# Optimization experiments

Measured on AMD Instinct MI355X. Metric: run time of the kernel, lower is better.

The kernel has to match this reference:

```python
import jax, jax.numpy as jnp
import numpy as np

B, S, D_IN, D_MODEL = 128, 2048, 512, 2048
M, NSY, H, T = 25, 64, 8, 10
REP = NSY * (NSY + 1) // 2
OUT_DIMS = S * 2
DH = D_IN // H
IU, JU = np.triu_indices(NSY)
IDX_OUT = np.arange(NSY)                      # 'first-last': first n neurons for out sync
IDX_ACT = np.arange(D_MODEL - NSY, D_MODEL)   # last n neurons for action sync


def _ln(x, g, b):
    mu = x.mean(-1, keepdims=True)
    var = x.var(-1, keepdims=True)
    return (x - mu) / jnp.sqrt(var + 1e-5) * g + b


def _sync(act, alpha, beta, r, idx):
    # pairwise upper-triangle outer product without materializing (B,n,n)
    sel = act[:, idx]
    pair = sel[:, IU] * sel[:, JU]  # (B, REP)
    if alpha is None:
        alpha, beta = pair, jnp.ones_like(pair)
    else:
        alpha = r * alpha + pair
        beta = r * beta + 1.0
    return alpha / jnp.sqrt(beta), alpha, beta


def _forward(tokens, emb, W_pos, b_pos, Wq, bq, Wk, bk, Wv, bv, Wo, bo, Ws, bs,
             ln_s_g, ln_s_b, ln_n_g, ln_n_b, Wn, bn, temp, Wout, bout,
             start_act, start_trace, decay_action, decay_out):
    # rotary-style learned positional embedding: rotate [0,1] by theta in [0,180deg]
    thetas = jnp.deg2rad(jnp.linspace(0.0, 180.0, S))
    rotated = jnp.stack([-jnp.sin(thetas), jnp.cos(thetas)], -1)  # (S,2)
    pe = rotated @ W_pos + b_pos                                   # (S, D_IN)
    feats = emb[tokens] + pe[None]                                 # (B,S,D_IN)
    kh = (feats @ Wk + bk).reshape(B, S, H, DH)
    vh = (feats @ Wv + bv).reshape(B, S, H, DH)
    r_a = jnp.exp(-decay_action)[None]
    r_o = jnp.exp(-decay_out)[None]
    act = jnp.broadcast_to(start_act[None], (B, D_MODEL))
    trace = jnp.broadcast_to(start_trace[None], (B, D_MODEL, M))
    a_a = b_a = a_o = b_o = None
    preds, certs = [], []
    for _ in range(T):
        s_act, a_a, b_a = _sync(act, a_a, b_a, r_a, IDX_ACT)
        q = (s_act @ Wq + bq).reshape(B, H, DH)
        scores = jnp.einsum('bhd,bshd->bhs', q, kh) / np.float32(np.sqrt(DH))
        attn = jax.nn.softmax(scores, -1)
        o = jnp.einsum('bhs,bshd->bhd', attn, vh).reshape(B, D_IN) @ Wo + bo
        # SynapseNet: Linear -> GLU -> LayerNorm
        pre = jnp.concatenate([o, act], -1) @ Ws + bs
        g1, g2 = jnp.split(pre, 2, -1)
        state = _ln(g1 * jax.nn.sigmoid(g2), ln_s_g, ln_s_b)  # (B, D_MODEL)
        trace = jnp.concatenate([trace[:, :, 1:], state[:, :, None]], -1)
        # NLM: per-neuron linear over memory, GLU, temperature
        xn = _ln(trace, ln_n_g, ln_n_b)
        y = jnp.einsum('bnm,mon->bno', xn, Wn) + bn  # (B, D_MODEL, 2)
        act = (y[..., 0] * jax.nn.sigmoid(y[..., 1])) / temp
        s_out, a_o, b_o = _sync(act, a_o, b_o, r_o, IDX_OUT)
        pred = s_out @ Wout + bout  # (B, OUT_DIMS)
        preds.append(pred)
        logits = pred.reshape(B, S, 2)
        p = jax.nn.softmax(logits, -1)
        ent = -(p * jax.nn.log_softmax(logits, -1)).sum(-1) / np.float32(np.log(2.0))
        ne = ent.mean(-1)
        certs.append(jnp.stack([ne, 1.0 - ne], -1))
    return jnp.stack(preds, -1), jnp.stack(certs, -1)  # (B,OUT_DIMS,T),(B,2,T)


def setup_inputs() -> dict:
    key = jax.random.key(0)
    ks = jax.random.split(key, 16)
    def n(k, shape, s=0.02):
        return (jax.random.normal(k, shape) * s).astype(jnp.float32)
    bound = 1.0 / np.sqrt(M + 2)
    return {
        'tokens': jax.random.randint(ks[0], (B, S), 0, 2, dtype=jnp.int32),
        'emb': n(ks[1], (2, D_IN), 1.0),
        'W_pos': n(ks[2], (2, D_IN)), 'b_pos': jnp.zeros((D_IN,)),
        'Wq': n(ks[3], (REP, D_IN)), 'bq': jnp.zeros((D_IN,)),
        'Wk': n(ks[4], (D_IN, D_IN)), 'bk': jnp.zeros((D_IN,)),
        'Wv': n(ks[5], (D_IN, D_IN)), 'bv': jnp.zeros((D_IN,)),
        'Wo': n(ks[6], (D_IN, D_IN)), 'bo': jnp.zeros((D_IN,)),
        'Ws': n(ks[7], (D_IN + D_MODEL, 2 * D_MODEL)), 'bs': jnp.zeros((2 * D_MODEL,)),
        'ln_s_g': jnp.ones((D_MODEL,)), 'ln_s_b': jnp.zeros((D_MODEL,)),
        'ln_n_g': jnp.ones((M,)), 'ln_n_b': jnp.zeros((M,)),
        'Wn': jax.random.uniform(ks[8], (M, 2, D_MODEL), minval=-bound, maxval=bound),
        'bn': jnp.zeros((1, D_MODEL, 2)),
        'temp': jnp.ones((1,)),
        'Wout': n(ks[9], (REP, OUT_DIMS)), 'bout': jnp.zeros((OUT_DIMS,)),
        'start_act': n(ks[10], (D_MODEL,), 1.0),
        'start_trace': n(ks[11], (D_MODEL, M), 1.0),
        'decay_action': jax.random.uniform(ks[12], (REP,), minval=0.0, maxval=1.0),
        'decay_out': jax.random.uniform(ks[13], (REP,), minval=0.0, maxval=1.0),
    }


def reference(tokens, emb, W_pos, b_pos, Wq, bq, Wk, bk, Wv, bv, Wo, bo, Ws, bs,
              ln_s_g, ln_s_b, ln_n_g, ln_n_b, Wn, bn, temp, Wout, bout,
              start_act, start_trace, decay_action, decay_out):
    return _forward(tokens, emb, W_pos, b_pos, Wq, bq, Wk, bk, Wv, bv, Wo, bo, Ws, bs,
                    ln_s_g, ln_s_b, ln_n_g, ln_n_b, Wn, bn, temp, Wout, bout,
                    start_act, start_trace, decay_action, decay_out)
```

## Files before the change

### kernel.cpp

```cpp
#include <hip/hip_runtime.h>
#include <hip/hip_bf16.h>
#include <math.h>

#define B_ 128
#define S_ 2048
#define D_IN_ 512
#define D_MODEL_ 2048
#define M_ 25
#define NSY_ 64
#define H_ 8
#define T_ 10
#define REP_ 2080
#define DH_ 64
#define PRED_N (B_ * 4096)

typedef unsigned short ushort_t;
typedef __bf16 bf16x8 __attribute__((ext_vector_type(8)));
typedef float f32x4 __attribute__((ext_vector_type(4)));
typedef unsigned short us8 __attribute__((ext_vector_type(8)));

__device__ __forceinline__ ushort_t f2bf(float f) {
    __hip_bfloat16 h = __float2bfloat16(f);
    return *(ushort_t*)&h;
}

__global__ __launch_bounds__(256) void gemm_bf16(
    const float* __restrict__ A, int lda,
    const ushort_t* __restrict__ Bt, int ldb,
    const float* __restrict__ bias,
    float* __restrict__ C, int ldc,
    int M, int N, int K, int kchunk)
{
    const int nb = blockIdx.x, mb = blockIdx.y, zb = blockIdx.z;
    const int k0 = zb * kchunk;
    const int k1 = min(K, k0 + kchunk);
    __shared__ ushort_t As[64][40];
    __shared__ ushort_t Bs[128][40];

    const int tid  = threadIdx.x;
    const int wave = tid >> 6;
    const int lane = tid & 63;
    const int quad = lane >> 4;
    const int mrow = lane & 15;

    f32x4 acc[4][2];
    #pragma unroll
    for (int s = 0; s < 4; s++)
        #pragma unroll
        for (int u = 0; u < 2; u++)
            acc[s][u] = (f32x4){0.f, 0.f, 0.f, 0.f};

    const int arow = tid >> 2, akc = (tid & 3) * 8;
    const int brow = tid >> 1, bkc = (tid & 1) * 16;

    for (int kk0 = k0; kk0 < k1; kk0 += 32) {
        {
            const float* ap = A + (size_t)(mb * 64 + arow) * lda + kk0 + akc;
            float4 v0 = *(const float4*)ap;
            float4 v1 = *(const float4*)(ap + 4);
            us8 w = { f2bf(v0.x), f2bf(v0.y), f2bf(v0.z), f2bf(v0.w),
                      f2bf(v1.x), f2bf(v1.y), f2bf(v1.z), f2bf(v1.w) };
            *(us8*)&As[arow][akc] = w;
        }
        {
            const ushort_t* bp = Bt + (size_t)(nb * 128 + brow) * ldb + kk0 + bkc;
            *(us8*)&Bs[brow][bkc]     = *(const us8*)bp;
            *(us8*)&Bs[brow][bkc + 8] = *(const us8*)(bp + 8);
        }
        __syncthreads();

        bf16x8 af[4], bfr[2];
        #pragma unroll
        for (int s = 0; s < 4; s++)
            af[s] = *(const bf16x8*)&As[s * 16 + mrow][quad * 8];
        #pragma unroll
        for (int u = 0; u < 2; u++)
            bfr[u] = *(const bf16x8*)&Bs[wave * 32 + u * 16 + mrow][quad * 8];
        #pragma unroll
        for (int s = 0; s < 4; s++)
            #pragma unroll
            for (int u = 0; u < 2; u++)
                acc[s][u] = __builtin_amdgcn_mfma_f32_16x16x32_bf16(
                    af[s], bfr[u], acc[s][u], 0, 0, 0);
        __syncthreads();
    }

    if (gridDim.z == 1) {
        #pragma unroll
        for (int s = 0; s < 4; s++)
            #pragma unroll
            for (int u = 0; u < 2; u++) {
                const int col = nb * 128 + wave * 32 + u * 16 + mrow;
                #pragma unroll
                for (int reg = 0; reg < 4; reg++) {
                    const int row = mb * 64 + s * 16 + quad * 4 + reg;
                    C[(size_t)row * ldc + col] = acc[s][u][reg] + bias[col];
                }
            }
    } else {
        #pragma unroll
        for (int s = 0; s < 4; s++)
            #pragma unroll
            for (int u = 0; u < 2; u++) {
                const int col = nb * 128 + wave * 32 + u * 16 + mrow;
                #pragma unroll
                for (int reg = 0; reg < 4; reg++) {
                    const int row = mb * 64 + s * 16 + quad * 4 + reg;
                    atomicAdd(&C[(size_t)row * ldc + col], acc[s][u][reg]);
                }
            }
    }
}

__global__ __launch_bounds__(256) void gemm_bb(
    const ushort_t* __restrict__ A, int lda,
    const ushort_t* __restrict__ Bt, int ldb,
    const float* __restrict__ bias,
    float* __restrict__ C, int ldc,
    int M, int N, int K, int kchunk)
{
    const int nb = blockIdx.x, mb = blockIdx.y, zb = blockIdx.z;
    const int k0 = zb * kchunk;
    const int k1 = min(K, k0 + kchunk);
    __shared__ ushort_t As[64][40];
    __shared__ ushort_t Bs[128][40];

    const int tid  = threadIdx.x;
    const int wave = tid >> 6;
    const int lane = tid & 63;
    const int quad = lane >> 4;
    const int mrow = lane & 15;

    f32x4 acc[4][2];
    #pragma unroll
    for (int s = 0; s < 4; s++)
        #pragma unroll
        for (int u = 0; u < 2; u++)
            acc[s][u] = (f32x4){0.f, 0.f, 0.f, 0.f};

    const int arow = tid >> 2, akc = (tid & 3) * 8;
    const int brow = tid >> 1, bkc = (tid & 1) * 16;

    for (int kk0 = k0; kk0 < k1; kk0 += 32) {
        {
            const ushort_t* ap = A + (size_t)(mb * 64 + arow) * lda + kk0 + akc;
            *(us8*)&As[arow][akc] = *(const us8*)ap;
        }
        {
            const ushort_t* bp = Bt + (size_t)(nb * 128 + brow) * ldb + kk0 + bkc;
            *(us8*)&Bs[brow][bkc]     = *(const us8*)bp;
            *(us8*)&Bs[brow][bkc + 8] = *(const us8*)(bp + 8);
        }
        __syncthreads();

        bf16x8 af[4], bfr[2];
        #pragma unroll
        for (int s = 0; s < 4; s++)
            af[s] = *(const bf16x8*)&As[s * 16 + mrow][quad * 8];
        #pragma unroll
        for (int u = 0; u < 2; u++)
            bfr[u] = *(const bf16x8*)&Bs[wave * 32 + u * 16 + mrow][quad * 8];
        #pragma unroll
        for (int s = 0; s < 4; s++)
            #pragma unroll
            for (int u = 0; u < 2; u++)
                acc[s][u] = __builtin_amdgcn_mfma_f32_16x16x32_bf16(
                    af[s], bfr[u], acc[s][u], 0, 0, 0);
        __syncthreads();
    }

    if (gridDim.z == 1) {
        #pragma unroll
        for (int s = 0; s < 4; s++)
            #pragma unroll
            for (int u = 0; u < 2; u++) {
                const int col = nb * 128 + wave * 32 + u * 16 + mrow;
                #pragma unroll
                for (int reg = 0; reg < 4; reg++) {
                    const int row = mb * 64 + s * 16 + quad * 4 + reg;
                    C[(size_t)row * ldc + col] = acc[s][u][reg] + bias[col];
                }
            }
    } else {
        #pragma unroll
        for (int s = 0; s < 4; s++)
            #pragma unroll
            for (int u = 0; u < 2; u++) {
                const int col = nb * 128 + wave * 32 + u * 16 + mrow;
                #pragma unroll
                for (int reg = 0; reg < 4; reg++) {
                    const int row = mb * 64 + s * 16 + quad * 4 + reg;
                    atomicAdd(&C[(size_t)row * ldc + col], acc[s][u][reg]);
                }
            }
    }
}

__global__ __launch_bounds__(256) void gemm_bb_dual(
    const ushort_t* __restrict__ A1, int lda1,
    const ushort_t* __restrict__ Bt1, int ldb1,
    float* __restrict__ C1, int ldc1, int kc1, int nb1x, int nblk1,
    const ushort_t* __restrict__ A2, int lda2,
    const ushort_t* __restrict__ Bt2, int ldb2,
    float* __restrict__ C2, int ldc2, int kc2, int nb2x)
{
    int bid = blockIdx.x;
    const ushort_t* A; const ushort_t* Bt; float* C;
    int lda, ldb, ldc, nb, mb, zb, kchunk;
    if (bid < nblk1) {
        A = A1; Bt = Bt1; C = C1; lda = lda1; ldb = ldb1; ldc = ldc1; kchunk = kc1;
        nb = bid % nb1x; mb = (bid / nb1x) & 1; zb = bid / (nb1x * 2);
    } else {
        bid -= nblk1;
        A = A2; Bt = Bt2; C = C2; lda = lda2; ldb = ldb2; ldc = ldc2; kchunk = kc2;
        nb = bid % nb2x; mb = (bid / nb2x) & 1; zb = bid / (nb2x * 2);
    }
    const int k0 = zb * kchunk;
    const int k1 = min(REP_, k0 + kchunk);
    __shared__ ushort_t As[64][40];
    __shared__ ushort_t Bs[128][40];

    const int tid  = threadIdx.x;
    const int wave = tid >> 6;
    const int lane = tid & 63;
    const int quad = lane >> 4;
    const int mrow = lane & 15;

    f32x4 acc[4][2];
    #pragma unroll
    for (int s = 0; s < 4; s++)
        #pragma unroll
        for (int u = 0; u < 2; u++)
            acc[s][u] = (f32x4){0.f, 0.f, 0.f, 0.f};

    const int arow = tid >> 2, akc = (tid & 3) * 8;
    const int brow = tid >> 1, bkc = (tid & 1) * 16;

    for (int kk0 = k0; kk0 < k1; kk0 += 32) {
        {
            const ushort_t* ap = A + (size_t)(mb * 64 + arow) * lda + kk0 + akc;
            *(us8*)&As[arow][akc] = *(const us8*)ap;
        }
        {
            const ushort_t* bp = Bt + (size_t)(nb * 128 + brow) * ldb + kk0 + bkc;
            *(us8*)&Bs[brow][bkc]     = *(const us8*)bp;
            *(us8*)&Bs[brow][bkc + 8] = *(const us8*)(bp + 8);
        }
        __syncthreads();

        bf16x8 af[4], bfr[2];
        #pragma unroll
        for (int s = 0; s < 4; s++)
            af[s] = *(const bf16x8*)&As[s * 16 + mrow][quad * 8];
        #pragma unroll
        for (int u = 0; u < 2; u++)
            bfr[u] = *(const bf16x8*)&Bs[wave * 32 + u * 16 + mrow][quad * 8];
        #pragma unroll
        for (int s = 0; s < 4; s++)
            #pragma unroll
            for (int u = 0; u < 2; u++)
                acc[s][u] = __builtin_amdgcn_mfma_f32_16x16x32_bf16(
                    af[s], bfr[u], acc[s][u], 0, 0, 0);
        __syncthreads();
    }

    #pragma unroll
    for (int s = 0; s < 4; s++)
        #pragma unroll
        for (int u = 0; u < 2; u++) {
            const int col = nb * 128 + wave * 32 + u * 16 + mrow;
            #pragma unroll
            for (int reg = 0; reg < 4; reg++) {
                const int row = mb * 64 + s * 16 + quad * 4 + reg;
                atomicAdd(&C[(size_t)row * ldc + col], acc[s][u][reg]);
            }
        }
}

__global__ __launch_bounds__(256) void gemm_qk(
    const float* __restrict__ q,
    const ushort_t* __restrict__ Kb,
    float* __restrict__ sc)
{
    const int nb = blockIdx.x, mb = blockIdx.y, z = blockIdx.z;
    const int c = z >> 3, h = z & 7;
    __shared__ ushort_t As[64][40];
    __shared__ ushort_t Bs[128][40];

    const int tid  = threadIdx.x;
    const int wave = tid >> 6;
    const int lane = tid & 63;
    const int quad = lane >> 4;
    const int mrow = lane & 15;

    f32x4 acc[4][2];
    #pragma unroll
    for (int s = 0; s < 4; s++)
        #pragma unroll
        for (int u = 0; u < 2; u++)
            acc[s][u] = (f32x4){0.f, 0.f, 0.f, 0.f};

    const int arow = tid >> 2, akc = (tid & 3) * 8;
    const int brow = tid >> 1, bkc = (tid & 1) * 16;
    const float* Abase = q + (size_t)h * 64;
    const ushort_t* Bbase = Kb + (size_t)c * S_ * 512 + h * 64;

    #pragma unroll
    for (int kk0 = 0; kk0 < 64; kk0 += 32) {
        {
            const float* ap = Abase + (size_t)(mb * 64 + arow) * 512 + kk0 + akc;
            float4 v0 = *(const float4*)ap;
            float4 v1 = *(const float4*)(ap + 4);
            us8 w = { f2bf(v0.x), f2bf(v0.y), f2bf(v0.z), f2bf(v0.w),
                      f2bf(v1.x), f2bf(v1.y), f2bf(v1.z), f2bf(v1.w) };
            *(us8*)&As[arow][akc] = w;
        }
        {
            const ushort_t* bp = Bbase + (size_t)(nb * 128 + brow) * 512 + kk0 + bkc;
            *(us8*)&Bs[brow][bkc]     = *(const us8*)bp;
            *(us8*)&Bs[brow][bkc + 8] = *(const us8*)(bp + 8);
        }
        __syncthreads();

        bf16x8 af[4], bfr[2];
        #pragma unroll
        for (int s = 0; s < 4; s++)
            af[s] = *(const bf16x8*)&As[s * 16 + mrow][quad * 8];
        #pragma unroll
        for (int u = 0; u < 2; u++)
            bfr[u] = *(const bf16x8*)&Bs[wave * 32 + u * 16 + mrow][quad * 8];
        #pragma unroll
        for (int s = 0; s < 4; s++)
            #pragma unroll
            for (int u = 0; u < 2; u++)
                acc[s][u] = __builtin_amdgcn_mfma_f32_16x16x32_bf16(
                    af[s], bfr[u], acc[s][u], 0, 0, 0);
        __syncthreads();
    }

    float* Cb = sc + (size_t)z * 128 * S_;
    #pragma unroll
    for (int s = 0; s < 4; s++)
        #pragma unroll
        for (int u = 0; u < 2; u++) {
            const int col = nb * 128 + wave * 32 + u * 16 + mrow;
            #pragma unroll
            for (int reg = 0; reg < 4; reg++) {
                const int row = mb * 64 + s * 16 + quad * 4 + reg;
                Cb[(size_t)row * S_ + col] = 0.125f * acc[s][u][reg];
            }
        }
}

__global__ __launch_bounds__(256) void attn_soft(
    const float* __restrict__ sc,
    const int*   __restrict__ tokens,
    ushort_t* __restrict__ P,
    float* __restrict__ o,
    float* __restrict__ cat,
    const float* __restrict__ bo,
    const float* __restrict__ bs,
    float* __restrict__ pre)
{
    const int bh = blockIdx.x;
    const int b = bh >> 3, h = bh & 7;
    __shared__ float red[256];
    const int tid = threadIdx.x;

    if (bh < 256) {
        const int idx = bh * 256 + tid;
        cat[(size_t)(idx >> 9) * 2560 + (idx & 511)] = bo[idx & 511];
    } else if (bh < 320) {
        const int idx = (bh - 256) * 256 + tid;
        *(float4*)&o[idx * 4] = make_float4(0.f, 0.f, 0.f, 0.f);
    } else if (bh < 832) {
        const int idx = (bh - 320) * 256 + tid;
        const float4* bs4 = (const float4*)bs;
        ((float4*)pre)[idx] = bs4[idx & 1023];
    }

    const float* sc0 = sc + ((size_t)h * 128 + b) * S_;
    const float* sc1 = sc + ((size_t)(8 + h) * 128 + b) * S_;
    const int* trow = tokens + (size_t)b * S_;

    int tok[8]; float sel[8];
    float lmax = -1e30f;
    #pragma unroll
    for (int i = 0; i < 8; i++) {
        const int s = tid + i * 256;
        tok[i] = trow[s];
        sel[i] = tok[i] ? sc1[s] : sc0[s];
        lmax = fmaxf(lmax, sel[i]);
    }
    red[tid] = lmax; __syncthreads();
    for (int off = 128; off > 0; off >>= 1) {
        if (tid < off) red[tid] = fmaxf(red[tid], red[tid + off]);
        __syncthreads();
    }
    const float mx = red[0];
    __syncthreads();

    float e[8];
    float lsum = 0.f;
    #pragma unroll
    for (int i = 0; i < 8; i++) {
        e[i] = expf(sel[i] - mx);
        lsum += e[i];
    }
    red[tid] = lsum; __syncthreads();
    for (int off = 128; off > 0; off >>= 1) {
        if (tid < off) red[tid] += red[tid + off];
        __syncthreads();
    }
    const float inv = 1.f / red[0];

    ushort_t* Pb = P + ((size_t)h * 128 + b) * 4096;
    #pragma unroll
    for (int i = 0; i < 8; i++) {
        const int s = tid + i * 256;
        const unsigned p = (unsigned)f2bf(e[i] * inv);
        const unsigned word = tok[i] ? (p << 16) : p;
        *(unsigned*)&Pb[s * 2] = word;
    }
}

__global__ __launch_bounds__(256) void gemm_pv(
    const ushort_t* __restrict__ P,
    const ushort_t* __restrict__ VT,
    float* __restrict__ o)
{
    const int mb = blockIdx.x, h = blockIdx.y, zb = blockIdx.z;
    const int k0 = zb * 512;
    __shared__ ushort_t As[64][40];
    __shared__ ushort_t Bs[64][40];

    const int tid  = threadIdx.x;
    const int wave = tid >> 6;
    const int lane = tid & 63;
    const int quad = lane >> 4;
    const int mrow = lane & 15;

    f32x4 acc[4];
    #pragma unroll
    for (int s = 0; s < 4; s++) acc[s] = (f32x4){0.f, 0.f, 0.f, 0.f};

    const int row = tid >> 2, kc = (tid & 3) * 8;
    const ushort_t* Ab = P  + ((size_t)h * 128 + mb * 64 + row) * 4096;
    const ushort_t* Bb = VT + ((size_t)h * 64 + row) * 4096;

    for (int kk = k0; kk < k0 + 512; kk += 32) {
        *(us8*)&As[row][kc] = *(const us8*)(Ab + kk + kc);
        *(us8*)&Bs[row][kc] = *(const us8*)(Bb + kk + kc);
        __syncthreads();
        bf16x8 bfr = *(const bf16x8*)&Bs[wave * 16 + mrow][quad * 8];
        #pragma unroll
        for (int s = 0; s < 4; s++) {
            bf16x8 af = *(const bf16x8*)&As[s * 16 + mrow][quad * 8];
            acc[s] = __builtin_amdgcn_mfma_f32_16x16x32_bf16(af, bfr, acc[s], 0, 0, 0);
        }
        __syncthreads();
    }

    const int col = h * 64 + wave * 16 + mrow;
    #pragma unroll
    for (int s = 0; s < 4; s++)
        #pragma unroll
        for (int reg = 0; reg < 4; reg++) {
            const int rowi = mb * 64 + s * 16 + quad * 4 + reg;
            atomicAdd(&o[(size_t)rowi * 512 + col], acc[s][reg]);
        }
}

__global__ void build_vt(const float* __restrict__ Vtab, ushort_t* __restrict__ VT)
{
    const int gid = blockIdx.x * 256 + threadIdx.x;
    const int k = gid & 4095;
    const int d = (gid >> 12) & 63;
    const int h = gid >> 18;
    const int s = k >> 1, c = k & 1;
    VT[gid] = f2bf(Vtab[((size_t)(c * S_ + s)) * 512 + h * 64 + d]);
}

__global__ void build_sync_tabs(const float* __restrict__ dec_act,
                                const float* __restrict__ dec_out,
                                int* __restrict__ ijtab,
                                float* __restrict__ r_act,
                                float* __restrict__ r_out,
                                float* __restrict__ sqb_act,
                                float* __restrict__ sqb_out)
{
    const int p = blockIdx.x * 256 + threadIdx.x;
    if (p >= REP_) return;
    int i = 0, rem = p;
    while (rem >= NSY_ - i) { rem -= NSY_ - i; i++; }
    ijtab[p] = (i << 16) | (i + rem);
    const float ra = expf(-dec_act[p]);
    const float ro = expf(-dec_out[p]);
    r_act[p] = ra; r_out[p] = ro;
    float ba = 1.f, bo2 = 1.f;
    sqb_act[p] = 1.f;
    sqb_out[p] = 1.f;
    for (int t = 1; t < T_; t++) {
        ba  = ra * ba  + 1.f;
        bo2 = ro * bo2 + 1.f;
        sqb_act[(size_t)t * REP_ + p] = sqrtf(ba);
        sqb_out[(size_t)t * REP_ + p] = sqrtf(bo2);
    }
}

__global__ __launch_bounds__(256) void transpose_bf16_kernel(
    const float* __restrict__ in, ushort_t* __restrict__ out, int K, int N)
{
    __shared__ float tile[32][33];
    const int k0 = blockIdx.y * 32, n0 = blockIdx.x * 32;
    const int tx = threadIdx.x & 31, ty4 = (threadIdx.x >> 5) * 4;
    #pragma unroll
    for (int i = 0; i < 4; i++)
        tile[ty4 + i][tx] = in[(size_t)(k0 + ty4 + i) * N + n0 + tx];
    __syncthreads();
    #pragma unroll
    for (int i = 0; i < 4; i++)
        out[(size_t)(n0 + ty4 + i) * K + k0 + tx] = f2bf(tile[tx][ty4 + i]);
}

__global__ void cast_bf16_kernel(const float* __restrict__ src,
                                 __hip_bfloat16* __restrict__ dst, int n)
{
    const int gid = (blockIdx.x * 256 + threadIdx.x) * 4;
    if (gid >= n) return;
    float4 v = *(const float4*)(src + gid);
    dst[gid + 0] = __float2bfloat16(v.x);
    dst[gid + 1] = __float2bfloat16(v.y);
    dst[gid + 2] = __float2bfloat16(v.z);
    dst[gid + 3] = __float2bfloat16(v.w);
}

__global__ void feats_kernel(const float* __restrict__ emb,
                             const float* __restrict__ Wp,
                             const float* __restrict__ bp,
                             float* __restrict__ f2)
{
    const int gid = blockIdx.x * 256 + threadIdx.x;
    const int k = gid & 511;
    const int s = (gid >> 9) & (S_ - 1);
    const int c = gid >> 20;
    const float th = 3.14159265358979323846f * (float)s / (float)(S_ - 1);
    f2[gid] = emb[c * 512 + k] + (-sinf(th)) * Wp[k] + cosf(th) * Wp[512 + k] + bp[k];
}

__global__ void init_act_kernel(const float* __restrict__ sa,
                                float* __restrict__ act,
                                float* __restrict__ cat)
{
    const int gid = blockIdx.x * 256 + threadIdx.x;
    const int b = gid >> 11, n = gid & 2047;
    const float v = sa[n];
    act[gid] = v;
    cat[(size_t)b * 2560 + 512 + n] = v;
}

__global__ void init_trace_kernel(const float* __restrict__ st,
                                  float* __restrict__ trace)
{
    const int gid = blockIdx.x * 256 + threadIdx.x;
    trace[gid] = st[gid % (D_MODEL_ * M_)];
}

__global__ void sync_kernel(const float* __restrict__ act,
                            float* __restrict__ alpha,
                            const float* __restrict__ decay,
                            const int t, const int off,
                            ushort_t* __restrict__ sout,
                            float* __restrict__ ib1, const float* __restrict__ bias1, int iN1,
                            float* __restrict__ ib2, const float* __restrict__ bias2, int iN2)
{
    const int b = blockIdx.x;
    const int tid = threadIdx.x;
    if (blockIdx.y == 8) {
        if (ib1)
            for (int n = tid; n < iN1; n += 256)
                ib1[(size_t)b * iN1 + n] = bias1[n];
        if (ib2)
            for (int n = tid; n < iN2; n += 256)
                ib2[(size_t)b * iN2 + n] = bias2[n];
    }
    const int p = blockIdx.y * 256 + tid;
    if (p >= REP_) return;
    int i = 0, rem = p;
    while (rem >= NSY_ - i) { rem -= NSY_ - i; i++; }
    const int j = i + rem;
    const float si = act[(size_t)b * D_MODEL_ + off + i];
    const float sj = act[(size_t)b * D_MODEL_ + off + j];
    const float pair = si * sj;
    const float r = expf(-decay[p]);
    float a;
    if (t == 0) a = pair;
    else        a = r * alpha[(size_t)b * REP_ + p] + pair;
    alpha[(size_t)b * REP_ + p] = a;
    float bta = 1.f;
    for (int k = 0; k < t; k++) bta = r * bta + 1.f;
    sout[(size_t)b * REP_ + p] = f2bf(a / sqrtf(bta));
}

__global__ __launch_bounds__(512, 2) void state_trace_kernel(
    const float* __restrict__ pre,
    const float* __restrict__ g,
    const float* __restrict__ bt,
    float* __restrict__ trace,
    const float* __restrict__ ln_g,
    const float* __restrict__ ln_b,
    const float* __restrict__ Wn,
    const float* __restrict__ bn,
    const float* __restrict__ temp,
    float* __restrict__ act,
    float* __restrict__ cat,
    const int t,
    const int* __restrict__ ijtab,
    const float* __restrict__ r_out,
    const float* __restrict__ sqb_out,
    float* __restrict__ a_o,
    ushort_t* __restrict__ s_outb,
    const float* __restrict__ bout,
    float* __restrict__ predt,
    const float* __restrict__ r_act,
    const float* __restrict__ sqb_act,
    float* __restrict__ a_a,
    ushort_t* __restrict__ s_actb,
    const float* __restrict__ bq,
    float* __restrict__ qbuf,
    const int do_act)
{
    const int b = blockIdx.x >> 1, half = blockIdx.x & 1;
    const int tid = threadIdx.x;
    __shared__ float v[D_MODEL_];
    __shared__ float r1[512], r2[512];
    __shared__ float sh_sync[64];
    float s1 = 0.f, s2 = 0.f;
    #pragma unroll
    for (int i = 0; i < 4; i++) {
        const int dd = tid + i * 512;
        const float g1 = pre[(size_t)b * 4096 + dd];
        const float g2 = pre[(size_t)b * 4096 + 2048 + dd];
        const float val = g1 * (1.f / (1.f + expf(-g2)));
        v[dd] = val; s1 += val; s2 += val * val;
    }
    r1[tid] = s1; r2[tid] = s2; __syncthreads();
    for (int off = 256; off > 0; off >>= 1) {
        if (tid < off) { r1[tid] += r1[tid + off]; r2[tid] += r2[tid + off]; }
        __syncthreads();
    }
    const float mu = r1[0] * (1.f / D_MODEL_);
    const float var = fmaxf(r2[0] * (1.f / D_MODEL_) - mu * mu, 0.f);
    const float sinv = 1.f / sqrtf(var + 1e-5f);
    const float tval = temp[0];

    #pragma unroll
    for (int i = 0; i < 2; i++) {
        const int n = half * 1024 + i * 512 + tid;
        const float sval = (v[n] - mu) * sinv * g[n] + bt[n];
        const int gid = b * 2048 + n;
        float* tr = trace + (size_t)gid * M_;
        float x[M_];
        #pragma unroll
        for (int m = 0; m < M_ - 1; m++) x[m] = tr[m + 1];
        x[M_ - 1] = sval;
        #pragma unroll
        for (int m = 0; m < M_; m++) tr[m] = x[m];
        float t1 = 0.f, t2 = 0.f;
        #pragma unroll
        for (int m = 0; m < M_; m++) { t1 += x[m]; t2 += x[m] * x[m]; }
        const float tmu = t1 * (1.f / M_);
        const float tvar = fmaxf(t2 * (1.f / M_) - tmu * tmu, 0.f);
        const float tinv = 1.f / sqrtf(tvar + 1e-5f);
        float y0 = bn[n * 2 + 0], y1 = bn[n * 2 + 1];
        #pragma unroll
        for (int m = 0; m < M_; m++) {
            const float xn = (x[m] - tmu) * tinv * ln_g[m] + ln_b[m];
            y0 += xn * Wn[(size_t)(m * 2 + 0) * D_MODEL_ + n];
            y1 += xn * Wn[(size_t)(m * 2 + 1) * D_MODEL_ + n];
        }
        const float a = y0 * (1.f / (1.f + expf(-y1))) / tval;
        act[gid] = a;
        cat[(size_t)b * 2560 + 512 + n] = a;
        if (half == 0) {
            if (i == 0 && tid < 64) sh_sync[tid] = a;
        } else {
            if (i == 1 && tid >= 448) sh_sync[tid - 448] = a;
        }
    }
    __syncthreads();

    if (half == 0) {
        for (int p = tid; p < REP_; p += 512) {
            const int ij = ijtab[p];
            const float pair = sh_sync[ij >> 16] * sh_sync[ij & 0xffff];
            const float r = r_out[p];
            float a2;
            if (t == 0) a2 = pair;
            else        a2 = r * a_o[(size_t)b * REP_ + p] + pair;
            a_o[(size_t)b * REP_ + p] = a2;
            s_outb[(size_t)b * REP_ + p] = f2bf(a2 / sqb_out[(size_t)t * REP_ + p]);
        }
        const float4* b4 = (const float4*)bout;
        float4* pd = (float4*)(predt + (size_t)b * 4096);
        for (int idx = tid; idx < 1024; idx += 512) pd[idx] = b4[idx];
    } else if (do_act) {
        for (int p = tid; p < REP_; p += 512) {
            const int ij = ijtab[p];
            const float pair = sh_sync[ij >> 16] * sh_sync[ij & 0xffff];
            const float r = r_act[p];
            float a2 = r * a_a[(size_t)b * REP_ + p] + pair;
            a_a[(size_t)b * REP_ + p] = a2;
            s_actb[(size_t)b * REP_ + p] = f2bf(a2 / sqb_act[(size_t)(t + 1) * REP_ + p]);
        }
        const float4* b4 = (const float4*)bq;
        float4* qb = (float4*)(qbuf + (size_t)b * 512);
        if (tid < 128) qb[tid] = b4[tid];
    }
}

__global__ __launch_bounds__(256) void ent_all_kernel(
    const float* __restrict__ predst,
    float* __restrict__ certbf)
{
    const int t = blockIdx.x >> 7;
    const int b = blockIdx.x & 127;
    const int tid = threadIdx.x;
    __shared__ float red[256];
    const float* pr = predst + (size_t)t * PRED_N + (size_t)b * 4096;
    float sum = 0.f;
    #pragma unroll
    for (int i = 0; i < 8; i++) {
        const int s = tid + i * 256;
        const float l0 = pr[2 * s], l1 = pr[2 * s + 1];
        const float mm = fmaxf(l0, l1);
        const float z0 = expf(l0 - mm), z1 = expf(l1 - mm);
        const float Z = z0 + z1;
        const float lz = logf(Z);
        const float p0 = z0 / Z, p1 = z1 / Z;
        const float lp0 = (l0 - mm) - lz, lp1 = (l1 - mm) - lz;
        sum += -(p0 * lp0 + p1 * lp1) * 1.4426950408889634f;
    }
    red[tid] = sum; __syncthreads();
    for (int off = 128; off > 0; off >>= 1) {
        if (tid < off) red[tid] += red[tid + off];
        __syncthreads();
    }
    if (tid == 0) {
        const float ne = red[0] * (1.f / S_);
        certbf[(size_t)t * B_ * 2 + b * 2 + 0] = ne;
        certbf[(size_t)t * B_ * 2 + b * 2 + 1] = 1.f - ne;
    }
}

__global__ __launch_bounds__(256) void finalize_kernel(
    const float* __restrict__ predstage,
    const float* __restrict__ certbuf,
    float* __restrict__ dout)
{
    __shared__ float tile[T_][1024];
    const int tid = threadIdx.x;
    const int row0 = blockIdx.x * 1024;
    #pragma unroll
    for (int t = 0; t < T_; t++) {
        float4 v = *(const float4*)(predstage + (size_t)t * PRED_N + row0 + tid * 4);
        tile[t][tid * 4 + 0] = v.x; tile[t][tid * 4 + 1] = v.y;
        tile[t][tid * 4 + 2] = v.z; tile[t][tid * 4 + 3] = v.w;
    }
    __syncthreads();
    float buf[40];
    #pragma unroll
    for (int r = 0; r < 4; r++)
        #pragma unroll
        for (int t = 0; t < T_; t++)
            buf[r * 10 + t] = tile[t][tid * 4 + r];
    float* dst = dout + (size_t)(row0 + tid * 4) * T_;
    #pragma unroll
    for (int k = 0; k < 10; k++)
        *(float4*)(dst + k * 4) = make_float4(buf[4*k], buf[4*k+1], buf[4*k+2], buf[4*k+3]);

    if (blockIdx.x == 0 && tid < B_) {
        const int b = tid;
        const size_t base = (size_t)PRED_N * T_;
        #pragma unroll
        for (int t = 0; t < T_; t++) {
            dout[base + (size_t)(b * 2 + 0) * T_ + t] = certbuf[t * B_ * 2 + b * 2 + 0];
            dout[base + (size_t)(b * 2 + 1) * T_ + t] = certbuf[t * B_ * 2 + b * 2 + 1];
        }
    }
}

extern "C" void kernel_launch(void* const* d_in, const int* in_sizes, int n_in,
                              void* d_out, int out_size, void* d_ws, size_t ws_size,
                              hipStream_t stream)
{
    const int*   tokens    = (const int*)  d_in[0];
    const float* emb       = (const float*)d_in[1];
    const float* W_pos     = (const float*)d_in[2];
    const float* b_pos     = (const float*)d_in[3];
    const float* Wq        = (const float*)d_in[4];
    const float* bq        = (const float*)d_in[5];
    const float* Wk        = (const float*)d_in[6];
    const float* bk        = (const float*)d_in[7];
    const float* Wv        = (const float*)d_in[8];
    const float* bv        = (const float*)d_in[9];
    const float* Wo        = (const float*)d_in[10];
    const float* bo        = (const float*)d_in[11];
    const float* Ws        = (const float*)d_in[12];
    const float* bs        = (const float*)d_in[13];
    const float* ln_s_g    = (const float*)d_in[14];
    const float* ln_s_b    = (const float*)d_in[15];
    const float* ln_n_g    = (const float*)d_in[16];
    const float* ln_n_b    = (const float*)d_in[17];
    const float* Wn        = (const float*)d_in[18];
    const float* bn        = (const float*)d_in[19];
    const float* temp      = (const float*)d_in[20];
    const float* Wout      = (const float*)d_in[21];
    const float* bout      = (const float*)d_in[22];
    const float* start_act = (const float*)d_in[23];
    const float* start_tr  = (const float*)d_in[24];
    const float* dec_act   = (const float*)d_in[25];
    const float* dec_out   = (const float*)d_in[26];
    float* out = (float*)d_out;
    float* w = (float*)d_ws;

    size_t off = 0;
    float* f2     = w + off; off += (size_t)2 * S_ * 512;
    float* Ktab   = w + off; off += (size_t)2 * S_ * 512;
    float* Vtab   = w + off; off += (size_t)2 * S_ * 512;
    float* act    = w + off; off += (size_t)B_ * D_MODEL_;
    float* cat    = w + off; off += (size_t)B_ * 2560;
    float* a_a    = w + off; off += (size_t)B_ * REP_;
    float* a_o    = w + off; off += (size_t)B_ * REP_;
    float* qbuf   = w + off; off += (size_t)B_ * 512;
    float* o_attn = w + off; off += (size_t)B_ * 512;
    float* pre    = w + off; off += (size_t)B_ * 4096;
    float* trace  = w + off; off += (size_t)B_ * D_MODEL_ * M_;
    float* scbuf  = w + off; off += (size_t)16 * 128 * S_;
    float* predst = w + off; off += (size_t)T_ * PRED_N;
    float* certbf = w + off; off += (size_t)T_ * B_ * 2;
    ushort_t* s_actb = (ushort_t*)(w + off); off += (size_t)B_ * REP_ / 2;
    ushort_t* s_outb = (ushort_t*)(w + off); off += (size_t)B_ * REP_ / 2;
    __hip_bfloat16* Kb = (__hip_bfloat16*)(w + off); off += (size_t)S_ * 512;
    ushort_t* Pbuf  = (ushort_t*)(w + off); off += (size_t)8 * 128 * 4096 / 2;
    ushort_t* VT    = (ushort_t*)(w + off); off += (size_t)8 * 64 * 4096 / 2;
    ushort_t* WkT   = (ushort_t*)(w + off); off += (size_t)512 * 512 / 2;
    ushort_t* WvT   = (ushort_t*)(w + off); off += (size_t)512 * 512 / 2;
    ushort_t* WqT   = (ushort_t*)(w + off); off += (size_t)512 * REP_ / 2;
    ushort_t* WoT   = (ushort_t*)(w + off); off += (size_t)512 * 512 / 2;
    ushort_t* WsT   = (ushort_t*)(w + off); off += (size_t)4096 * 2560 / 2;
    ushort_t* WoutT = (ushort_t*)(w + off); off += (size_t)4096 * REP_ / 2;
    int*   ijtab = (int*)(w + off); off += REP_;
    float* r_actT = w + off; off += REP_;
    float* r_outT = w + off; off += REP_;
    float* sqb_a  = w + off; off += (size_t)T_ * REP_;
    float* sqb_o  = w + off; off += (size_t)T_ * REP_;

    feats_kernel<<<(2 * S_ * 512) / 256, 256, 0, stream>>>(emb, W_pos, b_pos, f2);
    init_act_kernel<<<(B_ * D_MODEL_) / 256, 256, 0, stream>>>(start_act, act, cat);
    init_trace_kernel<<<(B_ * D_MODEL_ * M_) / 256, 256, 0, stream>>>(start_tr, trace);
    build_sync_tabs<<<(REP_ + 255) / 256, 256, 0, stream>>>(
        dec_act, dec_out, ijtab, r_actT, r_outT, sqb_a, sqb_o);

    transpose_bf16_kernel<<<dim3(512 / 32, 512 / 32), 256, 0, stream>>>(Wk, WkT, 512, 512);
    transpose_bf16_kernel<<<dim3(512 / 32, 512 / 32), 256, 0, stream>>>(Wv, WvT, 512, 512);
    transpose_bf16_kernel<<<dim3(512 / 32, REP_ / 32), 256, 0, stream>>>(Wq, WqT, REP_, 512);
    transpose_bf16_kernel<<<dim3(512 / 32, 512 / 32), 256, 0, stream>>>(Wo, WoT, 512, 512);
    transpose_bf16_kernel<<<dim3(4096 / 32, 2560 / 32), 256, 0, stream>>>(Ws, WsT, 2560, 4096);
    transpose_bf16_kernel<<<dim3(4096 / 32, REP_ / 32), 256, 0, stream>>>(Wout, WoutT, REP_, 4096);

    gemm_bf16<<<dim3(512 / 128, (2 * S_) / 64, 1), 256, 0, stream>>>(
        f2, 512, WkT, 512, bk, Ktab, 512, 2 * S_, 512, 512, 512);
    gemm_bf16<<<dim3(512 / 128, (2 * S_) / 64, 1), 256, 0, stream>>>(
        f2, 512, WvT, 512, bv, Vtab, 512, 2 * S_, 512, 512, 512);
    cast_bf16_kernel<<<(2 * S_ * 512 / 4) / 256, 256, 0, stream>>>(Ktab, Kb, 2 * S_ * 512);
    build_vt<<<(8 * 64 * 4096) / 256, 256, 0, stream>>>(Vtab, VT);

    sync_kernel<<<dim3(B_, 9), 256, 0, stream>>>(
        act, a_a, dec_act, 0, D_MODEL_ - NSY_, s_actb,
        qbuf, bq, 512, nullptr, nullptr, 0);
    gemm_bb<<<dim3(512 / 128, 2, 13), 256, 0, stream>>>(
        s_actb, REP_, WqT, REP_, bq, qbuf, 512, B_, 512, REP_, 160);

    for (int t = 0; t < T_; t++) {
        gemm_qk<<<dim3(S_ / 128, 2, 16), 256, 0, stream>>>(
            qbuf, (const ushort_t*)Kb, scbuf);
        attn_soft<<<B_ * H_, 256, 0, stream>>>(
            scbuf, tokens, Pbuf, o_attn, cat, bo, bs, pre);
        gemm_pv<<<dim3(2, 8, 8), 256, 0, stream>>>(Pbuf, VT, o_attn);

        gemm_bf16<<<dim3(512 / 128, 2, 8), 256, 0, stream>>>(
            o_attn, 512, WoT, 512, bo, cat, 2560, B_, 512, 512, 64);

        gemm_bf16<<<dim3(4096 / 128, 2, 8), 256, 0, stream>>>(
            cat, 2560, WsT, 2560, bs, pre, 4096, B_, 4096, 2560, 320);

        float* predt = predst + (size_t)t * PRED_N;
        state_trace_kernel<<<B_ * 2, 512, 0, stream>>>(
            pre, ln_s_g, ln_s_b, trace, ln_n_g, ln_n_b, Wn, bn, temp, act, cat,
            t, ijtab,
            r_outT, sqb_o, a_o, s_outb, bout, predt,
            r_actT, sqb_a, a_a, s_actb, bq, qbuf, (t < T_ - 1) ? 1 : 0);

        const int blocks2 = (t < T_ - 1) ? 104 : 0;
        gemm_bb_dual<<<dim3(320 + blocks2), 256, 0, stream>>>(
            s_outb, REP_, WoutT, REP_, predt, 4096, 416, 32, 320,
            s_actb, REP_, WqT, REP_, qbuf, 512, 160, 4);
    }

    ent_all_kernel<<<T_ * B_, 256, 0, stream>>>(predst, certbf);
    finalize_kernel<<<PRED_N / 1024, 256, 0, stream>>>(predst, certbf, out);
}
```

Before: 1.216 ms.

## Fuse time-step loop into persistent megakernel with software grid barriers

```diff
diff --git a/kernel.cpp b/kernel.cpp
--- a/kernel.cpp
+++ b/kernel.cpp
@@ -24,6 +24,455 @@
     return *(ushort_t*)&h;
 }
 
+struct MegaArgs {
+    float* qbuf; const ushort_t* Kb; float* scbuf; const int* tokens;
+    ushort_t* Pbuf; const ushort_t* VT; float* o_attn; float* obuf;
+    const float* bo; const float* bs;
+    float* pre0; float* pre1;
+    const ushort_t* WoT; const ushort_t* WsT;
+    const float* ln_s_g; const float* ln_s_b; float* trace;
+    const float* ln_n_g; const float* ln_n_b; const float* Wn; const float* bn;
+    const float* temp;
+    ushort_t* actb;
+    const int* ijtab; const float* r_out; const float* sqb_out; float* a_o; ushort_t* s_outb;
+    const float* bout; float* predst;
+    const float* r_act; const float* sqb_act; float* a_a; ushort_t* s_actb; const float* bq;
+    const ushort_t* WoutT; const ushort_t* WqT;
+    unsigned* bcnt; unsigned* bflag;
+};
+
+__device__ __forceinline__ void gbar(unsigned* cnt, unsigned* flag, unsigned ep)
+{
+    __syncthreads();
+    if (threadIdx.x == 0) {
+        __threadfence();
+        const unsigned target = ep * gridDim.x;
+        unsigned arrived = __hip_atomic_fetch_add(cnt, 1u, __ATOMIC_RELAXED,
+                                                  __HIP_MEMORY_SCOPE_AGENT) + 1u;
+        if (arrived == target) {
+            __hip_atomic_store(flag, ep, __ATOMIC_RELEASE, __HIP_MEMORY_SCOPE_AGENT);
+        } else {
+            while (__hip_atomic_load(flag, __ATOMIC_ACQUIRE, __HIP_MEMORY_SCOPE_AGENT) < ep)
+                __builtin_amdgcn_s_sleep(8);
+        }
+        __threadfence();
+    }
+    __syncthreads();
+}
+
+
+template<bool AF32>
+__device__ __forceinline__ void g_tile128(
+    const void* Ap, int lda, const ushort_t* Bt, int ldb,
+    float* C, int ldc, int nb, int mb, int k0, int k1, char* smem, int tid)
+{
+    ushort_t (*As)[40] = (ushort_t(*)[40])smem;
+    ushort_t (*Bs)[40] = (ushort_t(*)[40])(smem + 64 * 40 * 2);
+    const int wave = tid >> 6;
+    const int lane = tid & 63;
+    const int quad = lane >> 4;
+    const int mrow = lane & 15;
+
+    f32x4 acc[4][2];
+    #pragma unroll
+    for (int s = 0; s < 4; s++)
+        #pragma unroll
+        for (int u = 0; u < 2; u++)
+            acc[s][u] = (f32x4){0.f, 0.f, 0.f, 0.f};
+
+    const int arow = tid >> 2, akc = (tid & 3) * 8;
+    const int brow = tid >> 1, bkc = (tid & 1) * 16;
+
+    for (int kk0 = k0; kk0 < k1; kk0 += 32) {
+        if (AF32) {
+            const float* ap = (const float*)Ap + (size_t)(mb * 64 + arow) * lda + kk0 + akc;
+            float4 v0 = *(const float4*)ap;
+            float4 v1 = *(const float4*)(ap + 4);
+            us8 w = { f2bf(v0.x), f2bf(v0.y), f2bf(v0.z), f2bf(v0.w),
+                      f2bf(v1.x), f2bf(v1.y), f2bf(v1.z), f2bf(v1.w) };
+            *(us8*)&As[arow][akc] = w;
+        } else {
+            const ushort_t* ap = (const ushort_t*)Ap + (size_t)(mb * 64 + arow) * lda + kk0 + akc;
+            *(us8*)&As[arow][akc] = *(const us8*)ap;
+        }
+        {
+            const ushort_t* bp = Bt + (size_t)(nb * 128 + brow) * ldb + kk0 + bkc;
+            *(us8*)&Bs[brow][bkc]     = *(const us8*)bp;
+            *(us8*)&Bs[brow][bkc + 8] = *(const us8*)(bp + 8);
+        }
+        __syncthreads();
+
+        bf16x8 af[4], bfr[2];
+        #pragma unroll
+        for (int s = 0; s < 4; s++)
+            af[s] = *(const bf16x8*)&As[s * 16 + mrow][quad * 8];
+        #pragma unroll
+        for (int u = 0; u < 2; u++)
+            bfr[u] = *(const bf16x8*)&Bs[wave * 32 + u * 16 + mrow][quad * 8];
+        #pragma unroll
+        for (int s = 0; s < 4; s++)
+            #pragma unroll
+            for (int u = 0; u < 2; u++)
+                acc[s][u] = __builtin_amdgcn_mfma_f32_16x16x32_bf16(
+                    af[s], bfr[u], acc[s][u], 0, 0, 0);
+        __syncthreads();
+    }
+
+    #pragma unroll
+    for (int s = 0; s < 4; s++)
+        #pragma unroll
+        for (int u = 0; u < 2; u++) {
+            const int col = nb * 128 + wave * 32 + u * 16 + mrow;
+            #pragma unroll
+            for (int reg = 0; reg < 4; reg++) {
+                const int row = mb * 64 + s * 16 + quad * 4 + reg;
+                atomicAdd(&C[(size_t)row * ldc + col], acc[s][u][reg]);
+            }
+        }
+}
+
+__device__ __forceinline__ void g_qk(
+    int vb, const float* q, const ushort_t* Kb, float* sc, char* smem, int tid)
+{
+    const int nb = vb & 15, mb = (vb >> 4) & 1, z = vb >> 5;
+    const int c = z >> 3, h = z & 7;
+    ushort_t (*As)[40] = (ushort_t(*)[40])smem;
+    ushort_t (*Bs)[40] = (ushort_t(*)[40])(smem + 64 * 40 * 2);
+    const int wave = tid >> 6;
+    const int lane = tid & 63;
+    const int quad = lane >> 4;
+    const int mrow = lane & 15;
+
+    f32x4 acc[4][2];
+    #pragma unroll
+    for (int s = 0; s < 4; s++)
+        #pragma unroll
+        for (int u = 0; u < 2; u++)
+            acc[s][u] = (f32x4){0.f, 0.f, 0.f, 0.f};
+
+    const int arow = tid >> 2, akc = (tid & 3) * 8;
+    const int brow = tid >> 1, bkc = (tid & 1) * 16;
+    const float* Abase = q + (size_t)h * 64;
+    const ushort_t* Bbase = Kb + (size_t)c * S_ * 512 + h * 64;
+
+    #pragma unroll
+    for (int kk0 = 0; kk0 < 64; kk0 += 32) {
+        {
+            const float* ap = Abase + (size_t)(mb * 64 + arow) * 512 + kk0 + akc;
+            float4 v0 = *(const float4*)ap;
+            float4 v1 = *(const float4*)(ap + 4);
+            us8 w = { f2bf(v0.x), f2bf(v0.y), f2bf(v0.z), f2bf(v0.w),
+                      f2bf(v1.x), f2bf(v1.y), f2bf(v1.z), f2bf(v1.w) };
+            *(us8*)&As[arow][akc] = w;
+        }
+        {
+            const ushort_t* bp = Bbase + (size_t)(nb * 128 + brow) * 512 + kk0 + bkc;
+            *(us8*)&Bs[brow][bkc]     = *(const us8*)bp;
+            *(us8*)&Bs[brow][bkc + 8] = *(const us8*)(bp + 8);
+        }
+        __syncthreads();
+
+        bf16x8 af[4], bfr[2];
+        #pragma unroll
+        for (int s = 0; s < 4; s++)
+            af[s] = *(const bf16x8*)&As[s * 16 + mrow][quad * 8];
+        #pragma unroll
+        for (int u = 0; u < 2; u++)
+            bfr[u] = *(const bf16x8*)&Bs[wave * 32 + u * 16 + mrow][quad * 8];
+        #pragma unroll
+        for (int s = 0; s < 4; s++)
+            #pragma unroll
+            for (int u = 0; u < 2; u++)
+                acc[s][u] = __builtin_amdgcn_mfma_f32_16x16x32_bf16(
+                    af[s], bfr[u], acc[s][u], 0, 0, 0);
+        __syncthreads();
+    }
+
+    float* Cb = sc + (size_t)z * 128 * S_;
+    #pragma unroll
+    for (int s = 0; s < 4; s++)
+        #pragma unroll
+        for (int u = 0; u < 2; u++) {
+            const int col = nb * 128 + wave * 32 + u * 16 + mrow;
+            #pragma unroll
+            for (int reg = 0; reg < 4; reg++) {
+                const int row = mb * 64 + s * 16 + quad * 4 + reg;
+                Cb[(size_t)row * S_ + col] = 0.125f * acc[s][u][reg];
+            }
+        }
+}
+
+__device__ __forceinline__ void g_soft(
+    int vb, const MegaArgs& A, float* pre_nxt, char* smem, int tid)
+{
+    float* red = (float*)smem;
+    const int b = vb >> 3, h = vb & 7;
+
+    if (vb < 512) {
+        const int idx = vb * 256 + tid;
+        const float4* bs4 = (const float4*)A.bs;
+        ((float4*)pre_nxt)[idx] = bs4[idx & 1023];
+    } else if (vb < 576) {
+        const int idx = (vb - 512) * 256 + tid;
+        ((float4*)A.o_attn)[idx] = make_float4(0.f, 0.f, 0.f, 0.f);
+    } else if (vb < 640) {
+        const int idx = (vb - 576) * 256 + tid;
+        const float4* bo4 = (const float4*)A.bo;
+        ((float4*)A.obuf)[idx] = bo4[idx & 127];
+    }
+
+    const float* sc0 = A.scbuf + ((size_t)h * 128 + b) * S_;
+    const float* sc1 = A.scbuf + ((size_t)(8 + h) * 128 + b) * S_;
+    const int* trow = A.tokens + (size_t)b * S_;
+
+    int tok[8]; float sel[8];
+    float lmax = -1e30f;
+    #pragma unroll
+    for (int i = 0; i < 8; i++) {
+        const int s = tid + i * 256;
+        tok[i] = trow[s];
+        sel[i] = tok[i] ? sc1[s] : sc0[s];
+        lmax = fmaxf(lmax, sel[i]);
+    }
+    red[tid] = lmax; __syncthreads();
+    for (int off = 128; off > 0; off >>= 1) {
+        if (tid < off) red[tid] = fmaxf(red[tid], red[tid + off]);
+        __syncthreads();
+    }
+    const float mx = red[0];
+    __syncthreads();
+
+    float e[8];
+    float lsum = 0.f;
+    #pragma unroll
+    for (int i = 0; i < 8; i++) {
+        e[i] = expf(sel[i] - mx);
+        lsum += e[i];
+    }
+    red[tid] = lsum; __syncthreads();
+    for (int off = 128; off > 0; off >>= 1) {
+        if (tid < off) red[tid] += red[tid + off];
+        __syncthreads();
+    }
+    const float inv = 1.f / red[0];
+
+    ushort_t* Pb = A.Pbuf + ((size_t)h * 128 + b) * 4096;
+    #pragma unroll
+    for (int i = 0; i < 8; i++) {
+        const int s = tid + i * 256;
+        const unsigned p = (unsigned)f2bf(e[i] * inv);
+        const unsigned word = tok[i] ? (p << 16) : p;
+        *(unsigned*)&Pb[s * 2] = word;
+    }
+    __syncthreads();
+}
+
+__device__ __forceinline__ void g_pv(
+    int vb, const ushort_t* P, const ushort_t* VT, float* o, char* smem, int tid)
+{
+    const int mb = vb & 1, h = (vb >> 1) & 7, zb = vb >> 4;
+    const int k0 = zb * 512;
+    ushort_t (*As)[40] = (ushort_t(*)[40])smem;
+    ushort_t (*Bs)[40] = (ushort_t(*)[40])(smem + 64 * 40 * 2);
+    const int wave = tid >> 6;
+    const int lane = tid & 63;
+    const int quad = lane >> 4;
+    const int mrow = lane & 15;
+
+    f32x4 acc[4];
+    #pragma unroll
+    for (int s = 0; s < 4; s++) acc[s] = (f32x4){0.f, 0.f, 0.f, 0.f};
+
+    const int row = tid >> 2, kc = (tid & 3) * 8;
+    const ushort_t* Ab = P  + ((size_t)h * 128 + mb * 64 + row) * 4096;
+    const ushort_t* Bb = VT + ((size_t)h * 64 + row) * 4096;
+
+    for (int kk = k0; kk < k0 + 512; kk += 32) {
+        *(us8*)&As[row][kc] = *(const us8*)(Ab + kk + kc);
+        *(us8*)&Bs[row][kc] = *(const us8*)(Bb + kk + kc);
+        __syncthreads();
+        bf16x8 bfr = *(const bf16x8*)&Bs[wave * 16 + mrow][quad * 8];
+        #pragma unroll
+        for (int s = 0; s < 4; s++) {
+            bf16x8 af = *(const bf16x8*)&As[s * 16 + mrow][quad * 8];
+            acc[s] = __builtin_amdgcn_mfma_f32_16x16x32_bf16(af, bfr, acc[s], 0, 0, 0);
+        }
+        __syncthreads();
+    }
+
+    const int col = h * 64 + wave * 16 + mrow;
+    #pragma unroll
+    for (int s = 0; s < 4; s++)
+        #pragma unroll
+        for (int reg = 0; reg < 4; reg++) {
+            const int rowi = mb * 64 + s * 16 + quad * 4 + reg;
+            atomicAdd(&o[(size_t)rowi * 512 + col], acc[s][reg]);
+        }
+}
+
+__device__ __forceinline__ void g_st(
+    int vb, int t, int do_act, const float* pre, float* predt,
+    const MegaArgs& A, char* smem, int tid)
+{
+    const int b = vb >> 2, q = vb & 3;
+    float* v   = (float*)smem;
+    float* r1  = v + 2048;
+    float* r2  = r1 + 256;
+    float* shs = r2 + 256;
+
+    float s1 = 0.f, s2 = 0.f;
+    #pragma unroll
+    for (int i = 0; i < 8; i++) {
+        const int dd = tid + i * 256;
+        const float g1 = pre[(size_t)b * 4096 + dd];
+        const float g2 = pre[(size_t)b * 4096 + 2048 + dd];
+        const float val = g1 * (1.f / (1.f + expf(-g2)));
+        v[dd] = val; s1 += val; s2 += val * val;
+    }
+    r1[tid] = s1; r2[tid] = s2; __syncthreads();
+    for (int off = 128; off > 0; off >>= 1) {
+        if (tid < off) { r1[tid] += r1[tid + off]; r2[tid] += r2[tid + off]; }
+        __syncthreads();
+    }
+    const float mu = r1[0] * (1.f / D_MODEL_);
+    const float var = fmaxf(r2[0] * (1.f / D_MODEL_) - mu * mu, 0.f);
+    const float sinv = 1.f / sqrtf(var + 1e-5f);
+    const float tval = A.temp[0];
+
+    #pragma unroll
+    for (int i = 0; i < 2; i++) {
+        const int n = q * 512 + i * 256 + tid;
+        const float sval = (v[n] - mu) * sinv * A.ln_s_g[n] + A.ln_s_b[n];
+        const int gid = b * 2048 + n;
+        float* tr = A.trace + (size_t)gid * M_;
+        float x[M_];
+        #pragma unroll
+        for (int m = 0; m < M_ - 1; m++) x[m] = tr[m + 1];
+        x[M_ - 1] = sval;
+        #pragma unroll
+        for (int m = 0; m < M_; m++) tr[m] = x[m];
+        float t1 = 0.f, t2 = 0.f;
+        #pragma unroll
+        for (int m = 0; m < M_; m++) { t1 += x[m]; t2 += x[m] * x[m]; }
+        const float tmu = t1 * (1.f / M_);
+        const float tvar = fmaxf(t2 * (1.f / M_) - tmu * tmu, 0.f);
+        const float tinv = 1.f / sqrtf(tvar + 1e-5f);
+        float y0 = A.bn[n * 2 + 0], y1 = A.bn[n * 2 + 1];
+        #pragma unroll
+        for (int m = 0; m < M_; m++) {
+            const float xn = (x[m] - tmu) * tinv * A.ln_n_g[m] + A.ln_n_b[m];
+            y0 += xn * A.Wn[(size_t)(m * 2 + 0) * D_MODEL_ + n];
+            y1 += xn * A.Wn[(size_t)(m * 2 + 1) * D_MODEL_ + n];
+        }
+        const float a = y0 * (1.f / (1.f + expf(-y1))) / tval;
+        A.actb[gid] = f2bf(a);
+        if (q == 0) {
+            if (i == 0 && tid < 64) shs[tid] = a;
+        } else if (q == 3) {
+            if (i == 1 && tid >= 192) shs[tid - 192] = a;
+        }
+    }
+    __syncthreads();
+
+    if (q == 0) {
+        for (int p = tid; p < REP_; p += 256) {
+            const int ij = A.ijtab[p];
+            const float pair = shs[ij >> 16] * shs[ij & 0xffff];
+            const float r = A.r_out[p];
+            float a2;
+            if (t == 0) a2 = pair;
+            else        a2 = r * A.a_o[(size_t)b * REP_ + p] + pair;
+            A.a_o[(size_t)b * REP_ + p] = a2;
+            A.s_outb[(size_t)b * REP_ + p] = f2bf(a2 / A.sqb_out[(size_t)t * REP_ + p]);
+        }
+        const float4* b4 = (const float4*)A.bout;
+        float4* pd = (float4*)(predt + (size_t)b * 4096);
+        for (int idx = tid; idx < 1024; idx += 256) pd[idx] = b4[idx];
+    } else if (q == 3 && do_act) {
+        for (int p = tid; p < REP_; p += 256) {
+            const int ij = A.ijtab[p];
+            const float pair = shs[ij >> 16] * shs[ij & 0xffff];
+            const float r = A.r_act[p];
+            float a2 = r * A.a_a[(size_t)b * REP_ + p] + pair;
+            A.a_a[(size_t)b * REP_ + p] = a2;
+            A.s_actb[(size_t)b * REP_ + p] = f2bf(a2 / A.sqb_act[(size_t)(t + 1) * REP_ + p]);
+        }
+        const float4* b4 = (const float4*)A.bq;
+        float4* qb = (float4*)(A.qbuf + (size_t)b * 512);
+        if (tid < 128) qb[tid] = b4[tid];
+    }
+    __syncthreads();
+}
+
+__global__ __launch_bounds__(256) void mega_kernel(MegaArgs A)
+{
+    __shared__ __align__(16) char smem[16384];
+    const int tid = threadIdx.x;
+    const int gsz = (int)gridDim.x;
+    unsigned ep = 0;
+
+    for (int t = 0; t < T_; t++) {
+        float* pre_cur = (t & 1) ? A.pre1 : A.pre0;
+        float* pre_nxt = (t & 1) ? A.pre0 : A.pre1;
+        float* predt = A.predst + (size_t)t * PRED_N;
+        const int do_act = (t < T_ - 1) ? 1 : 0;
+
+        for (int vb = blockIdx.x; vb < 512; vb += gsz)
+            g_qk(vb, A.qbuf, A.Kb, A.scbuf, smem, tid);
+        gbar(A.bcnt, A.bflag, ++ep);
+
+        for (int vb = blockIdx.x; vb < 1024; vb += gsz)
+            g_soft(vb, A, pre_nxt, smem, tid);
+        gbar(A.bcnt, A.bflag, ++ep);
+
+        for (int vb = blockIdx.x; vb < 128; vb += gsz)
+            g_pv(vb, A.Pbuf, A.VT, A.o_attn, smem, tid);
+        gbar(A.bcnt, A.bflag, ++ep);
+
+        for (int vb = blockIdx.x; vb < 64; vb += gsz) {
+            const int nb = vb & 3, mb = (vb >> 2) & 1, zb = vb >> 3;
+            g_tile128<true>(A.o_attn, 512, A.WoT, 512, A.obuf, 512,
+                            nb, mb, zb * 64, zb * 64 + 64, smem, tid);
+        }
+        gbar(A.bcnt, A.bflag, ++ep);
+
+        for (int vb = blockIdx.x; vb < 256; vb += gsz) {
+            const int nb = vb & 31, mb = (vb >> 5) & 1, zb = vb >> 6;
+            g_tile128<true>(A.obuf, 512, A.WsT, 2560, pre_cur, 4096,
+                            nb, mb, zb * 128, zb * 128 + 128, smem, tid);
+        }
+        gbar(A.bcnt, A.bflag, ++ep);
+
+        for (int vb = blockIdx.x; vb < 512; vb += gsz)
+            g_st(vb, t, do_act, pre_cur, predt, A, smem, tid);
+        gbar(A.bcnt, A.bflag, ++ep);
+
+        const int nvb7 = do_act ? 936 : 320;
+        for (int vb = blockIdx.x; vb < nvb7; vb += gsz) {
+            if (vb < 320) {
+                const int nb = vb & 31, mb = (vb >> 5) & 1, zb = vb >> 6;
+                const int k0 = zb * 416;
+                g_tile128<false>(A.s_outb, REP_, A.WoutT, REP_, predt, 4096,
+                                 nb, mb, k0, min(REP_, k0 + 416), smem, tid);
+            } else if (vb < 424) {
+                const int v2 = vb - 320;
+                const int nb = v2 & 3, mb = (v2 >> 2) & 1, zb = v2 >> 3;
+                const int k0 = zb * 160;
+                g_tile128<false>(A.s_actb, REP_, A.WqT, REP_, A.qbuf, 512,
+                                 nb, mb, k0, min(REP_, k0 + 160), smem, tid);
+            } else {
+                const int v3 = vb - 424;
+                const int nb = v3 & 31, mb = (v3 >> 5) & 1, zb = v3 >> 6;
+                const int k0 = zb * 256;
+                g_tile128<false>(A.actb, 2048, A.WsT + 512, 2560, pre_nxt, 4096,
+                                 nb, mb, k0, k0 + 256, smem, tid);
+            }
+        }
+        gbar(A.bcnt, A.bflag, ++ep);
+    }
+}
+
+
 __global__ __launch_bounds__(256) void gemm_bf16(
     const float* __restrict__ A, int lda,
     const ushort_t* __restrict__ Bt, int ldb,
@@ -196,323 +645,81 @@
     }
 }
 
-__global__ __launch_bounds__(256) void gemm_bb_dual(
-    const ushort_t* __restrict__ A1, int lda1,
-    const ushort_t* __restrict__ Bt1, int ldb1,
-    float* __restrict__ C1, int ldc1, int kc1, int nb1x, int nblk1,
-    const ushort_t* __restrict__ A2, int lda2,
-    const ushort_t* __restrict__ Bt2, int ldb2,
-    float* __restrict__ C2, int ldc2, int kc2, int nb2x)
+#define IA_FE 8192
+#define IA_AC (IA_FE + 1024)
+#define IA_TR (IA_AC + 6400)
+#define IA_SY (IA_TR + 9)
+#define IA_NB (IA_SY + 1)
+__global__ void init_all(const float* __restrict__ emb, const float* __restrict__ Wp,
+                         const float* __restrict__ bp, float* __restrict__ f2,
+                         const float* __restrict__ sa, float* __restrict__ act,
+                         ushort_t* __restrict__ actb,
+                         const float* __restrict__ st, float* __restrict__ trace,
+                         const float* __restrict__ dec_act, const float* __restrict__ dec_out,
+                         int* __restrict__ ijtab, float* __restrict__ r_act,
+                         float* __restrict__ r_out, float* __restrict__ sqb_a,
+                         float* __restrict__ sqb_o, unsigned* __restrict__ barst)
+{
+    const int vb = blockIdx.x, tid = threadIdx.x;
+    if (vb < IA_FE) {
+        const int gid = vb * 256 + tid;
+        const int k = gid & 511;
+        const int s = (gid >> 9) & (S_ - 1);
+        const int c = gid >> 20;
+        const float th = 3.14159265358979323846f * (float)s / (float)(S_ - 1);
+        f2[gid] = emb[c * 512 + k] + (-sinf(th)) * Wp[k] + cosf(th) * Wp[512 + k] + bp[k];
+    } else if (vb < IA_AC) {
+        const int gid = (vb - IA_FE) * 256 + tid;
+        const int n = gid & 2047;
+        const float v = sa[n];
+        act[gid] = v;
+        actb[gid] = f2bf(v);
+    } else if (vb < IA_TR) {
+        const int idx4 = (vb - IA_AC) * 256 + tid;
+        ((float4*)trace)[idx4] = ((const float4*)st)[idx4 % 12800];
+    } else if (vb < IA_SY) {
+        const int p = (vb - IA_TR) * 256 + tid;
+        if (p >= REP_) return;
+        int i = 0, rem = p;
+        while (rem >= NSY_ - i) { rem -= NSY_ - i; i++; }
+        ijtab[p] = (i << 16) | (i + rem);
+        const float ra = expf(-dec_act[p]);
+        const float ro = expf(-dec_out[p]);
+        r_act[p] = ra; r_out[p] = ro;
+        float ba = 1.f, bo2 = 1.f;
+        sqb_a[p] = 1.f;
+        sqb_o[p] = 1.f;
+        for (int t = 1; t < T_; t++) {
+            ba  = ra * ba  + 1.f;
+            bo2 = ro * bo2 + 1.f;
+            sqb_a[(size_t)t * REP_ + p] = sqrtf(ba);
+            sqb_o[(size_t)t * REP_ + p] = sqrtf(bo2);
+        }
+    } else {
+        if (tid < 32) barst[tid] = 0u;
+    }
+}
+
+__global__ __launch_bounds__(256) void transpose_all(
+    const float* __restrict__ Wk, ushort_t* __restrict__ WkT,
+    const float* __restrict__ Wv, ushort_t* __restrict__ WvT,
+    const float* __restrict__ Wq, ushort_t* __restrict__ WqT,
+    const float* __restrict__ Wo, ushort_t* __restrict__ WoT,
+    const float* __restrict__ Ws, ushort_t* __restrict__ WsT,
+    const float* __restrict__ Wout, ushort_t* __restrict__ WoutT)
 {
     int bid = blockIdx.x;
-    const ushort_t* A; const ushort_t* Bt; float* C;
-    int lda, ldb, ldc, nb, mb, zb, kchunk;
-    if (bid < nblk1) {
-        A = A1; Bt = Bt1; C = C1; lda = lda1; ldb = ldb1; ldc = ldc1; kchunk = kc1;
-        nb = bid % nb1x; mb = (bid / nb1x) & 1; zb = bid / (nb1x * 2);
-    } else {
-        bid -= nblk1;
-        A = A2; Bt = Bt2; C = C2; lda = lda2; ldb = ldb2; ldc = ldc2; kchunk = kc2;
-        nb = bid % nb2x; mb = (bid / nb2x) & 1; zb = bid / (nb2x * 2);
-    }
-    const int k0 = zb * kchunk;
-    const int k1 = min(REP_, k0 + kchunk);
-    __shared__ ushort_t As[64][40];
-    __shared__ ushort_t Bs[128][40];
-
-    const int tid  = threadIdx.x;
-    const int wave = tid >> 6;
-    const int lane = tid & 63;
-    const int quad = lane >> 4;
-    const int mrow = lane & 15;
-
-    f32x4 acc[4][2];
-    #pragma unroll
-    for (int s = 0; s < 4; s++)
-        #pragma unroll
-        for (int u = 0; u < 2; u++)
-            acc[s][u] = (f32x4){0.f, 0.f, 0.f, 0.f};
-
-    const int arow = tid >> 2, akc = (tid & 3) * 8;
-    const int brow = tid >> 1, bkc = (tid & 1) * 16;
-
-    for (int kk0 = k0; kk0 < k1; kk0 += 32) {
-        {
-            const ushort_t* ap = A + (size_t)(mb * 64 + arow) * lda + kk0 + akc;
-            *(us8*)&As[arow][akc] = *(const us8*)ap;
-        }
-        {
-            const ushort_t* bp = Bt + (size_t)(nb * 128 + brow) * ldb + kk0 + bkc;
-            *(us8*)&Bs[brow][bkc]     = *(const us8*)bp;
-            *(us8*)&Bs[brow][bkc + 8] = *(const us8*)(bp + 8);
-        }
-        __syncthreads();
-
-        bf16x8 af[4], bfr[2];
-        #pragma unroll
-        for (int s = 0; s < 4; s++)
-            af[s] = *(const bf16x8*)&As[s * 16 + mrow][quad * 8];
-        #pragma unroll
-        for (int u = 0; u < 2; u++)
-            bfr[u] = *(const bf16x8*)&Bs[wave * 32 + u * 16 + mrow][quad * 8];
-        #pragma unroll
-        for (int s = 0; s < 4; s++)
-            #pragma unroll
-            for (int u = 0; u < 2; u++)
-                acc[s][u] = __builtin_amdgcn_mfma_f32_16x16x32_bf16(
-                    af[s], bfr[u], acc[s][u], 0, 0, 0);
-        __syncthreads();
-    }
-
-    #pragma unroll
-    for (int s = 0; s < 4; s++)
-        #pragma unroll
-        for (int u = 0; u < 2; u++) {
-            const int col = nb * 128 + wave * 32 + u * 16 + mrow;
-            #pragma unroll
-            for (int reg = 0; reg < 4; reg++) {
-                const int row = mb * 64 + s * 16 + quad * 4 + reg;
-                atomicAdd(&C[(size_t)row * ldc + col], acc[s][u][reg]);
-            }
-        }
-}
-
-__global__ __launch_bounds__(256) void gemm_qk(
-    const float* __restrict__ q,
-    const ushort_t* __restrict__ Kb,
-    float* __restrict__ sc)
-{
-    const int nb = blockIdx.x, mb = blockIdx.y, z = blockIdx.z;
-    const int c = z >> 3, h = z & 7;
-    __shared__ ushort_t As[64][40];
-    __shared__ ushort_t Bs[128][40];
-
-    const int tid  = threadIdx.x;
-    const int wave = tid >> 6;
-    const int lane = tid & 63;
-    const int quad = lane >> 4;
-    const int mrow = lane & 15;
-
-    f32x4 acc[4][2];
-    #pragma unroll
-    for (int s = 0; s < 4; s++)
-        #pragma unroll
-        for (int u = 0; u < 2; u++)
-            acc[s][u] = (f32x4){0.f, 0.f, 0.f, 0.f};
-
-    const int arow = tid >> 2, akc = (tid & 3) * 8;
-    const int brow = tid >> 1, bkc = (tid & 1) * 16;
-    const float* Abase = q + (size_t)h * 64;
-    const ushort_t* Bbase = Kb + (size_t)c * S_ * 512 + h * 64;
-
-    #pragma unroll
-    for (int kk0 = 0; kk0 < 64; kk0 += 32) {
-        {
-            const float* ap = Abase + (size_t)(mb * 64 + arow) * 512 + kk0 + akc;
-            float4 v0 = *(const float4*)ap;
-            float4 v1 = *(const float4*)(ap + 4);
-            us8 w = { f2bf(v0.x), f2bf(v0.y), f2bf(v0.z), f2bf(v0.w),
-                      f2bf(v1.x), f2bf(v1.y), f2bf(v1.z), f2bf(v1.w) };
-            *(us8*)&As[arow][akc] = w;
-        }
-        {
-            const ushort_t* bp = Bbase + (size_t)(nb * 128 + brow) * 512 + kk0 + bkc;
-            *(us8*)&Bs[brow][bkc]     = *(const us8*)bp;
-            *(us8*)&Bs[brow][bkc + 8] = *(const us8*)(bp + 8);
-        }
-        __syncthreads();
-
-        bf16x8 af[4], bfr[2];
-        #pragma unroll
-        for (int s = 0; s < 4; s++)
-            af[s] = *(const bf16x8*)&As[s * 16 + mrow][quad * 8];
-        #pragma unroll
-        for (int u = 0; u < 2; u++)
-            bfr[u] = *(const bf16x8*)&Bs[wave * 32 + u * 16 + mrow][quad * 8];
-        #pragma unroll
-        for (int s = 0; s < 4; s++)
-            #pragma unroll
-            for (int u = 0; u < 2; u++)
-                acc[s][u] = __builtin_amdgcn_mfma_f32_16x16x32_bf16(
-                    af[s], bfr[u], acc[s][u], 0, 0, 0);
-        __syncthreads();
-    }
-
-    float* Cb = sc + (size_t)z * 128 * S_;
-    #pragma unroll
-    for (int s = 0; s < 4; s++)
-        #pragma unroll
-        for (int u = 0; u < 2; u++) {
-            const int col = nb * 128 + wave * 32 + u * 16 + mrow;
-            #pragma unroll
-            for (int reg = 0; reg < 4; reg++) {
-                const int row = mb * 64 + s * 16 + quad * 4 + reg;
-                Cb[(size_t)row * S_ + col] = 0.125f * acc[s][u][reg];
-            }
-        }
-}
-
-__global__ __launch_bounds__(256) void attn_soft(
-    const float* __restrict__ sc,
-    const int*   __restrict__ tokens,
-    ushort_t* __restrict__ P,
-    float* __restrict__ o,
-    float* __restrict__ cat,
-    const float* __restrict__ bo,
-    const float* __restrict__ bs,
-    float* __restrict__ pre)
-{
-    const int bh = blockIdx.x;
-    const int b = bh >> 3, h = bh & 7;
-    __shared__ float red[256];
-    const int tid = threadIdx.x;
-
-    if (bh < 256) {
-        const int idx = bh * 256 + tid;
-        cat[(size_t)(idx >> 9) * 2560 + (idx & 511)] = bo[idx & 511];
-    } else if (bh < 320) {
-        const int idx = (bh - 256) * 256 + tid;
-        *(float4*)&o[idx * 4] = make_float4(0.f, 0.f, 0.f, 0.f);
-    } else if (bh < 832) {
-        const int idx = (bh - 320) * 256 + tid;
-        const float4* bs4 = (const float4*)bs;
-        ((float4*)pre)[idx] = bs4[idx & 1023];
-    }
-
-    const float* sc0 = sc + ((size_t)h * 128 + b) * S_;
-    const float* sc1 = sc + ((size_t)(8 + h) * 128 + b) * S_;
-    const int* trow = tokens + (size_t)b * S_;
-
-    int tok[8]; float sel[8];
-    float lmax = -1e30f;
-    #pragma unroll
-    for (int i = 0; i < 8; i++) {
-        const int s = tid + i * 256;
-        tok[i] = trow[s];
-        sel[i] = tok[i] ? sc1[s] : sc0[s];
-        lmax = fmaxf(lmax, sel[i]);
-    }
-    red[tid] = lmax; __syncthreads();
-    for (int off = 128; off > 0; off >>= 1) {
-        if (tid < off) red[tid] = fmaxf(red[tid], red[tid + off]);
-        __syncthreads();
-    }
-    const float mx = red[0];
-    __syncthreads();
-
-    float e[8];
-    float lsum = 0.f;
-    #pragma unroll
-    for (int i = 0; i < 8; i++) {
-        e[i] = expf(sel[i] - mx);
-        lsum += e[i];
-    }
-    red[tid] = lsum; __syncthreads();
-    for (int off = 128; off > 0; off >>= 1) {
-        if (tid < off) red[tid] += red[tid + off];
-        __syncthreads();
-    }
-    const float inv = 1.f / red[0];
-
-    ushort_t* Pb = P + ((size_t)h * 128 + b) * 4096;
-    #pragma unroll
-    for (int i = 0; i < 8; i++) {
-        const int s = tid + i * 256;
-        const unsigned p = (unsigned)f2bf(e[i] * inv);
-        const unsigned word = tok[i] ? (p << 16) : p;
-        *(unsigned*)&Pb[s * 2] = word;
-    }
-}
-
-__global__ __launch_bounds__(256) void gemm_pv(
-    const ushort_t* __restrict__ P,
-    const ushort_t* __restrict__ VT,
-    float* __restrict__ o)
-{
-    const int mb = blockIdx.x, h = blockIdx.y, zb = blockIdx.z;
-    const int k0 = zb * 512;
-    __shared__ ushort_t As[64][40];
-    __shared__ ushort_t Bs[64][40];
-
-    const int tid  = threadIdx.x;
-    const int wave = tid >> 6;
-    const int lane = tid & 63;
-    const int quad = lane >> 4;
-    const int mrow = lane & 15;
-
-    f32x4 acc[4];
-    #pragma unroll
-    for (int s = 0; s < 4; s++) acc[s] = (f32x4){0.f, 0.f, 0.f, 0.f};
-
-    const int row = tid >> 2, kc = (tid & 3) * 8;
-    const ushort_t* Ab = P  + ((size_t)h * 128 + mb * 64 + row) * 4096;
-    const ushort_t* Bb = VT + ((size_t)h * 64 + row) * 4096;
-
-    for (int kk = k0; kk < k0 + 512; kk += 32) {
-        *(us8*)&As[row][kc] = *(const us8*)(Ab + kk + kc);
-        *(us8*)&Bs[row][kc] = *(const us8*)(Bb + kk + kc);
-        __syncthreads();
-        bf16x8 bfr = *(const bf16x8*)&Bs[wave * 16 + mrow][quad * 8];
-        #pragma unroll
-        for (int s = 0; s < 4; s++) {
-            bf16x8 af = *(const bf16x8*)&As[s * 16 + mrow][quad * 8];
-            acc[s] = __builtin_amdgcn_mfma_f32_16x16x32_bf16(af, bfr, acc[s], 0, 0, 0);
-        }
-        __syncthreads();
-    }
-
-    const int col = h * 64 + wave * 16 + mrow;
-    #pragma unroll
-    for (int s = 0; s < 4; s++)
-        #pragma unroll
-        for (int reg = 0; reg < 4; reg++) {
-            const int rowi = mb * 64 + s * 16 + quad * 4 + reg;
-            atomicAdd(&o[(size_t)rowi * 512 + col], acc[s][reg]);
-        }
-}
-
-__global__ void build_vt(const float* __restrict__ Vtab, ushort_t* __restrict__ VT)
-{
-    const int gid = blockIdx.x * 256 + threadIdx.x;
-    const int k = gid & 4095;
-    const int d = (gid >> 12) & 63;
-    const int h = gid >> 18;
-    const int s = k >> 1, c = k & 1;
-    VT[gid] = f2bf(Vtab[((size_t)(c * S_ + s)) * 512 + h * 64 + d]);
-}
-
-__global__ void build_sync_tabs(const float* __restrict__ dec_act,
-                                const float* __restrict__ dec_out,
-                                int* __restrict__ ijtab,
-                                float* __restrict__ r_act,
-                                float* __restrict__ r_out,
-                                float* __restrict__ sqb_act,
-                                float* __restrict__ sqb_out)
-{
-    const int p = blockIdx.x * 256 + threadIdx.x;
-    if (p >= REP_) return;
-    int i = 0, rem = p;
-    while (rem >= NSY_ - i) { rem -= NSY_ - i; i++; }
-    ijtab[p] = (i << 16) | (i + rem);
-    const float ra = expf(-dec_act[p]);
-    const float ro = expf(-dec_out[p]);
-    r_act[p] = ra; r_out[p] = ro;
-    float ba = 1.f, bo2 = 1.f;
-    sqb_act[p] = 1.f;
-    sqb_out[p] = 1.f;
-    for (int t = 1; t < T_; t++) {
-        ba  = ra * ba  + 1.f;
-        bo2 = ro * bo2 + 1.f;
-        sqb_act[(size_t)t * REP_ + p] = sqrtf(ba);
-        sqb_out[(size_t)t * REP_ + p] = sqrtf(bo2);
-    }
-}
-
-__global__ __launch_bounds__(256) void transpose_bf16_kernel(
-    const float* __restrict__ in, ushort_t* __restrict__ out, int K, int N)
-{
+    const float* in; ushort_t* out; int K, N;
+    if      (bid <   256) {              in = Wk;   out = WkT;   K = 512;  N = 512;  }
+    else if (bid <   512) { bid -=  256; in = Wv;   out = WvT;   K = 512;  N = 512;  }
+    else if (bid <  1552) { bid -=  512; in = Wq;   out = WqT;   K = 2080; N = 512;  }
+    else if (bid <  1808) { bid -= 1552; in = Wo;   out = WoT;   K = 512;  N = 512;  }
+    else if (bid < 12048) { bid -= 1808; in = Ws;   out = WsT;   K = 2560; N = 4096; }
+    else                  { bid -= 12048; in = Wout; out = WoutT; K = 2080; N = 4096; }
+    const int bxw = N >> 5;
+    const int bx = bid % bxw, by = bid / bxw;
     __shared__ float tile[32][33];
-    const int k0 = blockIdx.y * 32, n0 = blockIdx.x * 32;
+    const int k0 = by * 32, n0 = bx * 32;
     const int tx = threadIdx.x & 31, ty4 = (threadIdx.x >> 5) * 4;
     #pragma unroll
     for (int i = 0; i < 4; i++)
@@ -535,35 +742,14 @@
     dst[gid + 3] = __float2bfloat16(v.w);
 }
 
-__global__ void feats_kernel(const float* __restrict__ emb,
-                             const float* __restrict__ Wp,
-                             const float* __restrict__ bp,
-                             float* __restrict__ f2)
+__global__ void build_vt(const float* __restrict__ Vtab, ushort_t* __restrict__ VT)
 {
     const int gid = blockIdx.x * 256 + threadIdx.x;
-    const int k = gid & 511;
-    const int s = (gid >> 9) & (S_ - 1);
-    const int c = gid >> 20;
-    const float th = 3.14159265358979323846f * (float)s / (float)(S_ - 1);
-    f2[gid] = emb[c * 512 + k] + (-sinf(th)) * Wp[k] + cosf(th) * Wp[512 + k] + bp[k];
-}
-
-__global__ void init_act_kernel(const float* __restrict__ sa,
-                                float* __restrict__ act,
-                                float* __restrict__ cat)
-{
-    const int gid = blockIdx.x * 256 + threadIdx.x;
-    const int b = gid >> 11, n = gid & 2047;
-    const float v = sa[n];
-    act[gid] = v;
-    cat[(size_t)b * 2560 + 512 + n] = v;
-}
-
-__global__ void init_trace_kernel(const float* __restrict__ st,
-                                  float* __restrict__ trace)
-{
-    const int gid = blockIdx.x * 256 + threadIdx.x;
-    trace[gid] = st[gid % (D_MODEL_ * M_)];
+    const int k = gid & 4095;
+    const int d = (gid >> 12) & 63;
+    const int h = gid >> 18;
+    const int s = k >> 1, c = k & 1;
+    VT[gid] = f2bf(Vtab[((size_t)(c * S_ + s)) * 512 + h * 64 + d]);
 }
 
 __global__ void sync_kernel(const float* __restrict__ act,
@@ -600,123 +786,6 @@
     float bta = 1.f;
     for (int k = 0; k < t; k++) bta = r * bta + 1.f;
     sout[(size_t)b * REP_ + p] = f2bf(a / sqrtf(bta));
-}
-
-__global__ __launch_bounds__(512, 2) void state_trace_kernel(
-    const float* __restrict__ pre,
-    const float* __restrict__ g,
-    const float* __restrict__ bt,
-    float* __restrict__ trace,
-    const float* __restrict__ ln_g,
-    const float* __restrict__ ln_b,
-    const float* __restrict__ Wn,
-    const float* __restrict__ bn,
-    const float* __restrict__ temp,
-    float* __restrict__ act,
-    float* __restrict__ cat,
-    const int t,
-    const int* __restrict__ ijtab,
-    const float* __restrict__ r_out,
-    const float* __restrict__ sqb_out,
-    float* __restrict__ a_o,
-    ushort_t* __restrict__ s_outb,
-    const float* __restrict__ bout,
-    float* __restrict__ predt,
-    const float* __restrict__ r_act,
-    const float* __restrict__ sqb_act,
-    float* __restrict__ a_a,
-    ushort_t* __restrict__ s_actb,
-    const float* __restrict__ bq,
-    float* __restrict__ qbuf,
-    const int do_act)
-{
-    const int b = blockIdx.x >> 1, half = blockIdx.x & 1;
-    const int tid = threadIdx.x;
-    __shared__ float v[D_MODEL_];
-    __shared__ float r1[512], r2[512];
-    __shared__ float sh_sync[64];
-    float s1 = 0.f, s2 = 0.f;
-    #pragma unroll
-    for (int i = 0; i < 4; i++) {
-        const int dd = tid + i * 512;
-        const float g1 = pre[(size_t)b * 4096 + dd];
-        const float g2 = pre[(size_t)b * 4096 + 2048 + dd];
-        const float val = g1 * (1.f / (1.f + expf(-g2)));
-        v[dd] = val; s1 += val; s2 += val * val;
-    }
-    r1[tid] = s1; r2[tid] = s2; __syncthreads();
-    for (int off = 256; off > 0; off >>= 1) {
-        if (tid < off) { r1[tid] += r1[tid + off]; r2[tid] += r2[tid + off]; }
-        __syncthreads();
-    }
-    const float mu = r1[0] * (1.f / D_MODEL_);
-    const float var = fmaxf(r2[0] * (1.f / D_MODEL_) - mu * mu, 0.f);
-    const float sinv = 1.f / sqrtf(var + 1e-5f);
-    const float tval = temp[0];
-
-    #pragma unroll
-    for (int i = 0; i < 2; i++) {
-        const int n = half * 1024 + i * 512 + tid;
-        const float sval = (v[n] - mu) * sinv * g[n] + bt[n];
-        const int gid = b * 2048 + n;
-        float* tr = trace + (size_t)gid * M_;
-        float x[M_];
-        #pragma unroll
-        for (int m = 0; m < M_ - 1; m++) x[m] = tr[m + 1];
-        x[M_ - 1] = sval;
-        #pragma unroll
-        for (int m = 0; m < M_; m++) tr[m] = x[m];
-        float t1 = 0.f, t2 = 0.f;
-        #pragma unroll
-        for (int m = 0; m < M_; m++) { t1 += x[m]; t2 += x[m] * x[m]; }
-        const float tmu = t1 * (1.f / M_);
-        const float tvar = fmaxf(t2 * (1.f / M_) - tmu * tmu, 0.f);
-        const float tinv = 1.f / sqrtf(tvar + 1e-5f);
-        float y0 = bn[n * 2 + 0], y1 = bn[n * 2 + 1];
-        #pragma unroll
-        for (int m = 0; m < M_; m++) {
-            const float xn = (x[m] - tmu) * tinv * ln_g[m] + ln_b[m];
-            y0 += xn * Wn[(size_t)(m * 2 + 0) * D_MODEL_ + n];
-            y1 += xn * Wn[(size_t)(m * 2 + 1) * D_MODEL_ + n];
-        }
-        const float a = y0 * (1.f / (1.f + expf(-y1))) / tval;
-        act[gid] = a;
-        cat[(size_t)b * 2560 + 512 + n] = a;
-        if (half == 0) {
-            if (i == 0 && tid < 64) sh_sync[tid] = a;
-        } else {
-            if (i == 1 && tid >= 448) sh_sync[tid - 448] = a;
-        }
-    }
-    __syncthreads();
-
-    if (half == 0) {
-        for (int p = tid; p < REP_; p += 512) {
-            const int ij = ijtab[p];
-            const float pair = sh_sync[ij >> 16] * sh_sync[ij & 0xffff];
-            const float r = r_out[p];
-            float a2;
-            if (t == 0) a2 = pair;
-            else        a2 = r * a_o[(size_t)b * REP_ + p] + pair;
-            a_o[(size_t)b * REP_ + p] = a2;
-            s_outb[(size_t)b * REP_ + p] = f2bf(a2 / sqb_out[(size_t)t * REP_ + p]);
-        }
-        const float4* b4 = (const float4*)bout;
-        float4* pd = (float4*)(predt + (size_t)b * 4096);
-        for (int idx = tid; idx < 1024; idx += 512) pd[idx] = b4[idx];
-    } else if (do_act) {
-        for (int p = tid; p < REP_; p += 512) {
-            const int ij = ijtab[p];
-            const float pair = sh_sync[ij >> 16] * sh_sync[ij & 0xffff];
-            const float r = r_act[p];
-            float a2 = r * a_a[(size_t)b * REP_ + p] + pair;
-            a_a[(size_t)b * REP_ + p] = a2;
-            s_actb[(size_t)b * REP_ + p] = f2bf(a2 / sqb_act[(size_t)(t + 1) * REP_ + p]);
-        }
-        const float4* b4 = (const float4*)bq;
-        float4* qb = (float4*)(qbuf + (size_t)b * 512);
-        if (tid < 128) qb[tid] = b4[tid];
-    }
 }
 
 __global__ __launch_bounds__(256) void ent_all_kernel(
@@ -829,18 +898,20 @@
     float* Ktab   = w + off; off += (size_t)2 * S_ * 512;
     float* Vtab   = w + off; off += (size_t)2 * S_ * 512;
     float* act    = w + off; off += (size_t)B_ * D_MODEL_;
-    float* cat    = w + off; off += (size_t)B_ * 2560;
     float* a_a    = w + off; off += (size_t)B_ * REP_;
     float* a_o    = w + off; off += (size_t)B_ * REP_;
     float* qbuf   = w + off; off += (size_t)B_ * 512;
     float* o_attn = w + off; off += (size_t)B_ * 512;
-    float* pre    = w + off; off += (size_t)B_ * 4096;
+    float* obuf   = w + off; off += (size_t)B_ * 512;
+    float* pre0   = w + off; off += (size_t)B_ * 4096;
+    float* pre1   = w + off; off += (size_t)B_ * 4096;
     float* trace  = w + off; off += (size_t)B_ * D_MODEL_ * M_;
     float* scbuf  = w + off; off += (size_t)16 * 128 * S_;
     float* predst = w + off; off += (size_t)T_ * PRED_N;
     float* certbf = w + off; off += (size_t)T_ * B_ * 2;
     ushort_t* s_actb = (ushort_t*)(w + off); off += (size_t)B_ * REP_ / 2;
     ushort_t* s_outb = (ushort_t*)(w + off); off += (size_t)B_ * REP_ / 2;
+    ushort_t* actb   = (ushort_t*)(w + off); off += (size_t)B_ * D_MODEL_ / 2;
     __hip_bfloat16* Kb = (__hip_bfloat16*)(w + off); off += (size_t)S_ * 512;
     ushort_t* Pbuf  = (ushort_t*)(w + off); off += (size_t)8 * 128 * 4096 / 2;
     ushort_t* VT    = (ushort_t*)(w + off); off += (size_t)8 * 64 * 4096 / 2;
@@ -850,63 +921,62 @@
     ushort_t* WoT   = (ushort_t*)(w + off); off += (size_t)512 * 512 / 2;
     ushort_t* WsT   = (ushort_t*)(w + off); off += (size_t)4096 * 2560 / 2;
     ushort_t* WoutT = (ushort_t*)(w + off); off += (size_t)4096 * REP_ / 2;
-    int*   ijtab = (int*)(w + off); off += REP_;
+    int*   ijtab  = (int*)(w + off); off += REP_;
     float* r_actT = w + off; off += REP_;
     float* r_outT = w + off; off += REP_;
     float* sqb_a  = w + off; off += (size_t)T_ * REP_;
     float* sqb_o  = w + off; off += (size_t)T_ * REP_;
-
-    feats_kernel<<<(2 * S_ * 512) / 256, 256, 0, stream>>>(emb, W_pos, b_pos, f2);
-    init_act_kernel<<<(B_ * D_MODEL_) / 256, 256, 0, stream>>>(start_act, act, cat);
-    init_trace_kernel<<<(B_ * D_MODEL_ * M_) / 256, 256, 0, stream>>>(start_tr, trace);
-    build_sync_tabs<<<(REP_ + 255) / 256, 256, 0, stream>>>(
-        dec_act, dec_out, ijtab, r_actT, r_outT, sqb_a, sqb_o);
-
-    transpose_bf16_kernel<<<dim3(512 / 32, 512 / 32), 256, 0, stream>>>(Wk, WkT, 512, 512);
-    transpose_bf16_kernel<<<dim3(512 / 32, 512 / 32), 256, 0, stream>>>(Wv, WvT, 512, 512);
-    transpose_bf16_kernel<<<dim3(512 / 32, REP_ / 32), 256, 0, stream>>>(Wq, WqT, REP_, 512);
-    transpose_bf16_kernel<<<dim3(512 / 32, 512 / 32), 256, 0, stream>>>(Wo, WoT, 512, 512);
-    transpose_bf16_kernel<<<dim3(4096 / 32, 2560 / 32), 256, 0, stream>>>(Ws, WsT, 2560, 4096);
-    transpose_bf16_kernel<<<dim3(4096 / 32, REP_ / 32), 256, 0, stream>>>(Wout, WoutT, REP_, 4096);
-
-    gemm_bf16<<<dim3(512 / 128, (2 * S_) / 64, 1), 256, 0, stream>>>(
+    unsigned* barst = (unsigned*)(w + off); off += 32;
+
+    init_all<<<IA_NB, 256, 0, stream>>>(
+        emb, W_pos, b_pos, f2, start_act, act, actb, start_tr, trace,
+        dec_act, dec_out, ijtab, r_actT, r_outT, sqb_a, sqb_o, barst);
+    transpose_all<<<20368, 256, 0, stream>>>(
+        Wk, WkT, Wv, WvT, Wq, WqT, Wo, WoT, Ws, WsT, Wout, WoutT);
+    gemm_bf16<<<dim3(4, 64, 1), 256, 0, stream>>>(
         f2, 512, WkT, 512, bk, Ktab, 512, 2 * S_, 512, 512, 512);
-    gemm_bf16<<<dim3(512 / 128, (2 * S_) / 64, 1), 256, 0, stream>>>(
+    gemm_bf16<<<dim3(4, 64, 1), 256, 0, stream>>>(
         f2, 512, WvT, 512, bv, Vtab, 512, 2 * S_, 512, 512, 512);
     cast_bf16_kernel<<<(2 * S_ * 512 / 4) / 256, 256, 0, stream>>>(Ktab, Kb, 2 * S_ * 512);
     build_vt<<<(8 * 64 * 4096) / 256, 256, 0, stream>>>(Vtab, VT);
 
     sync_kernel<<<dim3(B_, 9), 256, 0, stream>>>(
         act, a_a, dec_act, 0, D_MODEL_ - NSY_, s_actb,
-        qbuf, bq, 512, nullptr, nullptr, 0);
-    gemm_bb<<<dim3(512 / 128, 2, 13), 256, 0, stream>>>(
+        qbuf, bq, 512, pre0, bs, 4096);
+    gemm_bb<<<dim3(32, 2, 8), 256, 0, stream>>>(
+        actb, 2048, WsT + 512, 2560, bq, pre0, 4096, B_, 4096, 2048, 256);
+    gemm_bb<<<dim3(4, 2, 13), 256, 0, stream>>>(
         s_actb, REP_, WqT, REP_, bq, qbuf, 512, B_, 512, REP_, 160);
 
-    for (int t = 0; t < T_; t++) {
-        gemm_qk<<<dim3(S_ / 128, 2, 16), 256, 0, stream>>>(
-            qbuf, (const ushort_t*)Kb, scbuf);
-        attn_soft<<<B_ * H_, 256, 0, stream>>>(
-            scbuf, tokens, Pbuf, o_attn, cat, bo, bs, pre);
-        gemm_pv<<<dim3(2, 8, 8), 256, 0, stream>>>(Pbuf, VT, o_attn);
-
-        gemm_bf16<<<dim3(512 / 128, 2, 8), 256, 0, stream>>>(
-            o_attn, 512, WoT, 512, bo, cat, 2560, B_, 512, 512, 64);
-
-        gemm_bf16<<<dim3(4096 / 128, 2, 8), 256, 0, stream>>>(
-            cat, 2560, WsT, 2560, bs, pre, 4096, B_, 4096, 2560, 320);
-
-        float* predt = predst + (size_t)t * PRED_N;
-        state_trace_kernel<<<B_ * 2, 512, 0, stream>>>(
-            pre, ln_s_g, ln_s_b, trace, ln_n_g, ln_n_b, Wn, bn, temp, act, cat,
-            t, ijtab,
-            r_outT, sqb_o, a_o, s_outb, bout, predt,
-            r_actT, sqb_a, a_a, s_actb, bq, qbuf, (t < T_ - 1) ? 1 : 0);
-
-        const int blocks2 = (t < T_ - 1) ? 104 : 0;
-        gemm_bb_dual<<<dim3(320 + blocks2), 256, 0, stream>>>(
-            s_outb, REP_, WoutT, REP_, predt, 4096, 416, 32, 320,
-            s_actb, REP_, WqT, REP_, qbuf, 512, 160, 4);
-    }
+    MegaArgs ma;
+    ma.qbuf = qbuf; ma.Kb = (const ushort_t*)Kb; ma.scbuf = scbuf; ma.tokens = tokens;
+    ma.Pbuf = Pbuf; ma.VT = VT; ma.o_attn = o_attn; ma.obuf = obuf;
+    ma.bo = bo; ma.bs = bs;
+    ma.pre0 = pre0; ma.pre1 = pre1;
+    ma.WoT = WoT; ma.WsT = WsT;
+    ma.ln_s_g = ln_s_g; ma.ln_s_b = ln_s_b; ma.trace = trace;
+    ma.ln_n_g = ln_n_g; ma.ln_n_b = ln_n_b; ma.Wn = Wn; ma.bn = bn;
+    ma.temp = temp;
+    ma.actb = actb;
+    ma.ijtab = ijtab; ma.r_out = r_outT; ma.sqb_out = sqb_o; ma.a_o = a_o; ma.s_outb = s_outb;
+    ma.bout = bout; ma.predst = predst;
+    ma.r_act = r_actT; ma.sqb_act = sqb_a; ma.a_a = a_a; ma.s_actb = s_actb; ma.bq = bq;
+    ma.WoutT = WoutT; ma.WqT = WqT;
+    ma.bcnt = barst; ma.bflag = barst + 16;
+
+    static int ncu = 0;
+    if (!ncu) {
+        hipDeviceProp_t prop;
+        if (hipGetDeviceProperties(&prop, 0) == hipSuccess) ncu = prop.multiProcessorCount;
+        if (ncu <= 0) ncu = 256;
+    }
+    int mab = 0;
+    hipOccupancyMaxActiveBlocksPerMultiprocessor(&mab, mega_kernel, 256, 0);
+    if (mab < 1) mab = 1;
+    long grid = (long)mab * ncu;
+    if (grid > 1024) grid = 1024;
+    if (grid < 1) grid = 1;
+    mega_kernel<<<dim3((int)grid), 256, 0, stream>>>(ma);
 
     ent_all_kernel<<<T_ * B_, 256, 0, stream>>>(predst, certbf);
     finalize_kernel<<<PRED_N / 1024, 256, 0, stream>>>(predst, certbf, out);
```

Result: slower. 3.444 ms (+183.1%).
